# Kernel tuning notes

Hardware: AMD Instinct MI355X
Metric: run time of the kernel (lower is better)

## Reference

```python
import jax, jax.numpy as jnp
import numpy as np

SQ3, SQ5, SQ15 = 3.0**0.5, 5.0**0.5, 15.0**0.5
M0, M1, M2 = 128, 64, 32
DIM = M0 + 3*M1 + 5*M2  # 480
N_GRAPHS, ATOMS_PER, N_BLOCKS = 512, 16, 8
N_NODES = N_GRAPHS * ATOMS_PER
N_EDGES = 100000
CUTOFF = 5.0
AVG_DEGREE = 15.57
AVG_NUM_NODES = 18.03
ATOM_MAP = np.array([-1, 0, -1, -1, -1, -1, 1, 2, 3, 4], dtype=np.int32)


def _sph(u):
    # component-normalized real spherical harmonics l=1,2 of unit vectors u [E,3]
    x, y, z = u[:, 0], u[:, 1], u[:, 2]
    sh1 = SQ3 * u
    sh2 = jnp.stack([SQ15*x*y, SQ15*y*z, 0.5*SQ5*(3.0*z*z - 1.0),
                     SQ15*x*z, 0.5*SQ15*(x*x - y*y)], axis=-1)
    return sh1, sh2


def _seg_softmax(logits, seg, n):
    m = jax.ops.segment_max(logits, seg, num_segments=n)
    e = jnp.exp(logits - m[seg])
    s = jax.ops.segment_sum(e, seg, num_segments=n)
    return e / (s[seg] + 1e-9)


def _energy(pos, fp, node_atom, edge_src, edge_dst, batch):
    (atom_table, rbf_centers, rbf_width, deg_W1, deg_W2, deg_W3,
     blk_Wv0, blk_Wv1, blk_Wv2, blk_Ws0, blk_Ws1, blk_Ws2,
     blk_rW1, blk_rW2, blk_rW3, blk_Wa_src, blk_Wa_dst, blk_Wa_e, blk_wa,
     blk_ff1, blk_ff2, blk_fg1, blk_fg2, blk_fW1, blk_fW2,
     ln_g, ln_b, head_W0, head_out) = fp
    N = pos.shape[0]
    mapped = jnp.asarray(ATOM_MAP)[node_atom]
    f0 = atom_table[mapped]                       # [N,128] scalar channels
    f1 = jnp.zeros((N, M1, 3), f0.dtype)
    f2 = jnp.zeros((N, M2, 5), f0.dtype)

    vec = pos[edge_src] - pos[edge_dst]           # [E,3]
    r = jnp.sqrt(jnp.sum(vec*vec, axis=1) + 1e-12)
    u = vec / r[:, None]
    sh1, sh2 = _sph(u)
    rbf = jnp.exp(-0.5 * ((r[:, None] - rbf_centers[None, :]) / rbf_width[None, :])**2)  # [E,128]

    # edge-degree embedding: radial-weighted SH scattered to dst, scaled by avg degree
    h = jax.nn.silu(rbf @ deg_W1)
    h = jax.nn.silu(h @ deg_W2)
    g = h @ deg_W3                                 # [E,224]
    g0, g1, g2 = g[:, :M0], g[:, M0:M0+M1], g[:, M0+M1:]
    inv = 1.0 / (AVG_DEGREE ** 0.5)
    f0 = f0 + inv * jax.ops.segment_sum(g0, edge_dst, num_segments=N)
    f1 = f1 + inv * jax.ops.segment_sum(g1[:, :, None]*sh1[:, None, :], edge_dst, num_segments=N)
    f2 = f2 + inv * jax.ops.segment_sum(g2[:, :, None]*sh2[:, None, :], edge_dst, num_segments=N)

    for i in range(N_BLOCKS):
        s0, s1, s2 = f0[edge_src], f1[edge_src], f2[edge_src]
        h = jax.nn.silu(rbf @ blk_rW1[i])
        h = jax.nn.silu(h @ blk_rW2[i])
        g = h @ blk_rW3[i]
        g0, g1, g2 = g[:, :M0], g[:, M0:M0+M1], g[:, M0+M1:]
        # equivariant tensor-product messages: value path (radial-gated) + SH-injection path
        m0 = (s0 @ blk_Wv0[i]) * g0 + s0 @ blk_Ws0[i]
        m1 = jnp.einsum('ecx,cd->edx', s1, blk_Wv1[i]) * g1[:, :, None] \
             + (s0 @ blk_Ws1[i])[:, :, None] * sh1[:, None, :]
        m2 = jnp.einsum('ecx,cd->edx', s2, blk_Wv2[i]) * g2[:, :, None] \
             + (s0 @ blk_Ws2[i])[:, :, None] * sh2[:, None, :]
        # scalar attention, softmax over incoming edges per destination node
        z = jnp.tanh(s0 @ blk_Wa_src[i] + f0[edge_dst] @ blk_Wa_dst[i] + h @ blk_Wa_e[i])
        a = _seg_softmax(z @ blk_wa[i], edge_dst, N)  # [E]
        f0 = f0 + jax.ops.segment_sum(a[:, None]*m0, edge_dst, num_segments=N)
        f1 = f1 + jax.ops.segment_sum(a[:, None, None]*m1, edge_dst, num_segments=N)
        f2 = f2 + jax.ops.segment_sum(a[:, None, None]*m2, edge_dst, num_segments=N)
        # equivariant FFN: scalar MLP + scalar-gated per-l channel mixing
        f0 = f0 + jax.nn.silu(f0 @ blk_ff1[i]) @ blk_ff2[i]
        f1 = f1 + jnp.einsum('ncx,cd->ndx', f1, blk_fW1[i]) * jax.nn.sigmoid(f0 @ blk_fg1[i])[:, :, None]
        f2 = f2 + jnp.einsum('ncx,cd->ndx', f2, blk_fW2[i]) * jax.nn.sigmoid(f0 @ blk_fg2[i])[:, :, None]

    flat = jnp.concatenate([f0, f1.reshape(N, 3*M1), f2.reshape(N, 5*M2)], axis=1)  # [N,480]
    mu = jnp.mean(flat, axis=1, keepdims=True)
    var = jnp.var(flat, axis=1, keepdims=True)
    flat = (flat - mu) * jax.lax.rsqrt(var + 1e-5) * ln_g + ln_b
    # head: only the 0e part can reach the final 1x0e output (equivariance)
    e_node = jax.nn.silu(flat[:, :M0] @ head_W0) @ head_out  # [N,1]
    energy = jax.ops.segment_sum(e_node[:, 0], batch, num_segments=N_GRAPHS) / (AVG_NUM_NODES ** 0.5)
    return energy  # [B]


def setup_inputs() -> dict:
    key = jax.random.key(0)
    rng = np.random.default_rng(0)
    B, A = N_GRAPHS, ATOMS_PER
    pos_np = rng.uniform(0.0, 6.0, size=(B, A, 3)).astype(np.float32)
    d = np.linalg.norm(pos_np[:, :, None, :] - pos_np[:, None, :, :], axis=-1)
    mask = (d < CUTOFF) & (d > 1e-6)
    gi, si, di = np.nonzero(mask)
    src = np.resize((gi*A + si).astype(np.int32), N_EDGES)
    dst = np.resize((gi*A + di).astype(np.int32), N_EDGES)
    atoms = rng.choice(np.array([1, 6, 7, 8, 9], dtype=np.int32), size=B*A)
    batch = np.repeat(np.arange(B, dtype=np.int32), A)

    ks = iter(jax.random.split(key, 40))
    def W(shape, fan):
        return jax.random.normal(next(ks), shape, jnp.float32) / np.sqrt(fan)
    D3 = M0 + M1 + M2  # 224
    return dict(
        pos=jnp.asarray(pos_np.reshape(B*A, 3)),
        atom_table=W((5, M0), 1.0),
        rbf_centers=jnp.linspace(0.0, CUTOFF, 128),
        rbf_width=jnp.full((128,), 0.25, jnp.float32),
        deg_W1=W((128, 64), 128), deg_W2=W((64, 64), 64), deg_W3=W((64, D3), 64),
        blk_Wv0=W((8, M0, M0), M0), blk_Wv1=W((8, M1, M1), M1), blk_Wv2=W((8, M2, M2), M2),
        blk_Ws0=W((8, M0, M0), M0), blk_Ws1=W((8, M0, M1), M0), blk_Ws2=W((8, M0, M2), M0),
        blk_rW1=W((8, 128, 64), 128), blk_rW2=W((8, 64, 64), 64), blk_rW3=W((8, 64, D3), 64),
        blk_Wa_src=W((8, M0, 32), M0), blk_Wa_dst=W((8, M0, 32), M0), blk_Wa_e=W((8, 64, 32), 64),
        blk_wa=W((8, 32), 32),
        blk_ff1=W((8, M0, 4*M0), M0), blk_ff2=W((8, 4*M0, M0), 4*M0),
        blk_fg1=W((8, M0, M1), M0), blk_fg2=W((8, M0, M2), M0),
        blk_fW1=W((8, M1, M1), M1), blk_fW2=W((8, M2, M2), M2),
        ln_g=jnp.ones((DIM,), jnp.float32), ln_b=jnp.zeros((DIM,), jnp.float32),
        head_W0=W((M0, M0), M0), head_out=W((M0, 1), M0),
        node_atom=jnp.asarray(atoms), edge_src=jnp.asarray(src),
        edge_dst=jnp.asarray(dst), batch=jnp.asarray(batch),
    )


def reference(pos, atom_table, rbf_centers, rbf_width, deg_W1, deg_W2, deg_W3,
              blk_Wv0, blk_Wv1, blk_Wv2, blk_Ws0, blk_Ws1, blk_Ws2,
              blk_rW1, blk_rW2, blk_rW3, blk_Wa_src, blk_Wa_dst, blk_Wa_e, blk_wa,
              blk_ff1, blk_ff2, blk_fg1, blk_fg2, blk_fW1, blk_fW2,
              ln_g, ln_b, head_W0, head_out,
              node_atom, edge_src, edge_dst, batch):
    fp = (atom_table, rbf_centers, rbf_width, deg_W1, deg_W2, deg_W3,
          blk_Wv0, blk_Wv1, blk_Wv2, blk_Ws0, blk_Ws1, blk_Ws2,
          blk_rW1, blk_rW2, blk_rW3, blk_Wa_src, blk_Wa_dst, blk_Wa_e, blk_wa,
          blk_ff1, blk_ff2, blk_fg1, blk_fg2, blk_fW1, blk_fW2,
          ln_g, ln_b, head_W0, head_out)

    def _tot(p):
        e = _energy(p, fp, node_atom, edge_src, edge_dst, batch)
        return jnp.sum(e), e

    (_, energy), gpos = jax.value_and_grad(_tot, has_aux=True)(pos)
    forces = -gpos  # dy = -dE/dpos, as in the torch autograd.grad call
    return energy, forces
```

## Files before the change

kernel.cpp:

```cpp
#include <hip/hip_runtime.h>
#include <string.h>
#include <math.h>

#define NE 100000
#define NN 8192
#define NG 512
#define CHF 25000
#define NF 4
#define CHB 20000
#define NB 5
#define CHIF 50000
#define NIF 2
#define CHIB 34000
#define NIB 3
#define NNC 8192

#define SQ3F  1.7320508075688772f
#define SQ5F  2.23606797749979f
#define SQ15F 3.872983346207417f

__constant__ int c_amap[10] = {-1,0,-1,-1,-1,-1,1,2,3,4};

typedef __attribute__((ext_vector_type(4))) float f32x4;
typedef __attribute__((ext_vector_type(8))) short bf16x8;

__device__ __forceinline__ float sigf(float x){ return 1.0f/(1.0f+expf(-x)); }
__device__ __forceinline__ float siluf(float x){ return x*sigf(x); }
__device__ __forceinline__ float dsiluf(float x){ float s=sigf(x); return s*(1.0f + x*(1.0f-s)); }

__device__ __forceinline__ float wred64(float v){
  #pragma unroll
  for (int o=32;o>0;o>>=1) v += __shfl_down(v,o,64);
  return v;
}
__device__ __forceinline__ int lbound(const int* a, int n, int v){
  int lo=0, hi=n;
  while (lo<hi){ int m=(lo+hi)>>1; if (a[m]<v) lo=m+1; else hi=m; }
  return lo;
}
__device__ __forceinline__ unsigned short f2b(float x){
  unsigned u=__float_as_uint(x);
  unsigned r=(u + 0x7fffu + ((u>>16)&1u))>>16;
  return (unsigned short)r;
}
__device__ __forceinline__ float b2f(unsigned short b){
  return __uint_as_float(((unsigned)b)<<16);
}

__global__ void k_hist(const int* keys, int* hist, int n){
  int i = blockIdx.x*256 + threadIdx.x;
  if (i < n) atomicAdd(&hist[keys[i]], 1);
}
__global__ __launch_bounds__(256) void k_scan0(const int* hist, int* rows){
  __shared__ int part[256];
  int t = threadIdx.x;
  int base = t*32;
  int loc[32];
  int s = 0;
  #pragma unroll
  for (int i=0;i<32;i++){ loc[i]=s; s+=hist[base+i]; }
  part[t]=s;
  __syncthreads();
  int pre=0;
  for (int i=0;i<t;i++) pre+=part[i];
  #pragma unroll
  for (int i=0;i<32;i++) rows[base+i]=pre+loc[i];
  if (t==255) rows[NN]=pre+s;
}
__global__ void k_fillperm(const int* keys, int* cursor, int* perm, int n){
  int i = blockIdx.x*256 + threadIdx.x;
  if (i < n){
    int slot = atomicAdd(&cursor[keys[i]], 1);
    perm[slot] = i;
  }
}
__global__ void k_mkedge(const int* perm, const int* src, const int* dst, int* src2, int* dst2){
  int k = blockIdx.x*256 + threadIdx.x;
  if (k < NE){ int e = perm[k]; src2[k] = src[e]; dst2[k] = dst[e]; }
}

__global__ void k_wcat(const float* Wv0,const float* Ws0,const float* Ws1,const float* Ws2, float* W){
  int t = blockIdx.x*256 + threadIdx.x;
  if (t >= 8*128*352) return;
  int i = t/45056, r = t - i*45056;
  int k = r/352, n = r - k*352;
  float v;
  if (n < 128) v = Wv0[(size_t)i*16384 + k*128 + n];
  else if (n < 256) v = Ws0[(size_t)i*16384 + k*128 + (n-128)];
  else if (n < 320) v = Ws1[(size_t)i*8192 + k*64 + (n-256)];
  else v = Ws2[(size_t)i*4096 + k*32 + (n-320)];
  W[t] = v;
}
__global__ void k_wcatz(const float* WaS,const float* WaD,const float* WaE, float* W){
  int t = blockIdx.x*256 + threadIdx.x;
  if (t >= 8*320*32) return;
  int i = t/10240, r = t - i*10240;
  int k = r/32, c = r - k*32;
  float v;
  if (k < 128) v = WaS[(size_t)i*4096 + k*32 + c];
  else if (k < 256) v = WaD[(size_t)i*4096 + (k-128)*32 + c];
  else v = WaE[(size_t)i*2048 + (k-256)*32 + c];
  W[t] = v;
}
__global__ void k_wcatg(const float* fg1,const float* fg2, float* W){
  int t = blockIdx.x*256 + threadIdx.x;
  if (t >= 8*128*96) return;
  int i = t/12288, r = t - i*12288;
  int k = r/96, c = r - k*96;
  float v;
  if (c < 64) v = fg1[(size_t)i*8192 + k*64 + c];
  else v = fg2[(size_t)i*4096 + k*32 + (c-64)];
  W[t] = v;
}

template<int MT, bool TB, bool ACC, int ACT, bool GATHER, bool SPLIT, bool ARBF, bool DMUL, bool PREOUT>
__global__ __launch_bounds__(256) void k_mgemm(
    const float* __restrict__ A, const int* __restrict__ idx,
    const float* __restrict__ B, float* __restrict__ C,
    int M, int Nd, int K,
    const float* __restrict__ cen, const float* __restrict__ wid,
    const float* __restrict__ dm, float* __restrict__ pre)
{
  constexpr int TPR = 256/MT;
  constexpr int EPT = 32/TPR;
  constexpr int RT  = MT/16;
  __shared__ unsigned short Asb[(SPLIT?2:1)*MT*40];
  __shared__ unsigned short Btb[(SPLIT?2:1)*2560];
  const int bm = blockIdx.x*MT, bn = blockIdx.y*64;
  const int tid = threadIdx.x;
  const int wave = tid>>6, lane = tid&63;
  const int arow_s = tid / TPR, aoff = (tid % TPR) * EPT;
  const int bsrow = tid>>2, bsoff = (tid&3)*8;
  f32x4 acc[RT];
  #pragma unroll
  for (int r=0;r<RT;r++) acc[r] = (f32x4){0.f,0.f,0.f,0.f};
  int arow = -1;
  {
    int gr = bm + arow_s;
    if (gr < M) arow = GATHER ? idx[gr] : gr;
  }
  int bcol = bn + bsrow;
  for (int k0=0;k0<K;k0+=32){
    #pragma unroll
    for (int i=0;i<EPT;i++){
      float v = 0.0f;
      if (arow>=0){
        if (ARBF){
          float r = A[arow];
          int kk = k0 + aoff + i;
          float t = (r - cen[kk]) / wid[kk];
          v = expf(-0.5f*t*t);
        } else {
          v = A[(size_t)arow*K + k0 + aoff + i];
        }
      }
      unsigned short h = f2b(v);
      Asb[arow_s*40 + aoff + i] = h;
      if (SPLIT) Asb[MT*40 + arow_s*40 + aoff + i] = f2b(v - b2f(h));
    }
    #pragma unroll
    for (int i=0;i<8;i++){
      float v = 0.0f;
      if (bcol < Nd) v = TB ? B[(size_t)bcol*K + k0 + bsoff + i] : B[(size_t)(k0+bsoff+i)*Nd + bcol];
      unsigned short h = f2b(v);
      Btb[bsrow*40 + bsoff + i] = h;
      if (SPLIT) Btb[2560 + bsrow*40 + bsoff + i] = f2b(v - b2f(h));
    }
    __syncthreads();
    int boff = (wave*16 + (lane&15))*40 + (lane>>4)*8;
    bf16x8 bh = *(const bf16x8*)&Btb[boff];
    #pragma unroll
    for (int r=0;r<RT;r++){
      int aoff2 = (r*16 + (lane&15))*40 + (lane>>4)*8;
      bf16x8 ah = *(const bf16x8*)&Asb[aoff2];
      acc[r] = __builtin_amdgcn_mfma_f32_16x16x32_bf16(ah, bh, acc[r], 0,0,0);
      if (SPLIT){
        bf16x8 bl = *(const bf16x8*)&Btb[2560 + boff];
        bf16x8 al = *(const bf16x8*)&Asb[MT*40 + aoff2];
        acc[r] = __builtin_amdgcn_mfma_f32_16x16x32_bf16(ah, bl, acc[r], 0,0,0);
        acc[r] = __builtin_amdgcn_mfma_f32_16x16x32_bf16(al, bh, acc[r], 0,0,0);
      }
    }
    __syncthreads();
  }
  int col = bn + wave*16 + (lane&15);
  if (col < Nd){
    #pragma unroll
    for (int r=0;r<RT;r++){
      #pragma unroll
      for (int v=0;v<4;v++){
        int row = bm + r*16 + (lane>>4)*4 + v;
        if (row >= M) continue;
        size_t o = (size_t)row*Nd + col;
        float x = acc[r][v];
        if (ACC) x += C[o];
        if (DMUL) x *= dsiluf(dm[o]);
        if (PREOUT) pre[o] = x;
        if (ACT == 1) x = siluf(x);
        else if (ACT == 2) x = tanhf(x);
        else if (ACT == 3) x = sigf(x);
        C[o] = x;
      }
    }
  }
}

template<bool SPLIT, bool LAMB>
__global__ __launch_bounds__(256) void k_zgemm(
    const float* __restrict__ F0, const int* __restrict__ sidx, const int* __restrict__ didx,
    const float* __restrict__ H2v, const float* __restrict__ WZ, const float* __restrict__ wa,
    float* __restrict__ Zc, float* __restrict__ LAM, int M)
{
  __shared__ unsigned short Asb[(SPLIT?2:1)*64*40];
  __shared__ unsigned short Btb[(SPLIT?2:1)*2560];
  __shared__ float lacc[128];
  const int bm = blockIdx.x*64;
  const int tid = threadIdx.x, wave = tid>>6, lane = tid&63;
  const int arow_s = tid>>2, aoff = (tid&3)*8;
  const int bsrow = tid>>2, bsoff = (tid&3)*8;
  f32x4 acc[4];
  #pragma unroll
  for (int r=0;r<4;r++) acc[r] = (f32x4){0.f,0.f,0.f,0.f};
  long sb=-1, db=-1, hb=-1;
  {
    int gr = bm + arow_s;
    if (gr < M){ sb=(long)sidx[gr]*128; db=(long)didx[gr]*128; hb=(long)gr*64; }
  }
  for (int k0=0;k0<320;k0+=32){
    long ab; int rk; const float* sp;
    if (k0 < 128){ ab=sb; rk=k0; sp=F0; }
    else if (k0 < 256){ ab=db; rk=k0-128; sp=F0; }
    else { ab=hb; rk=k0-256; sp=H2v; }
    #pragma unroll
    for (int i=0;i<8;i++){
      float v = (ab>=0) ? sp[ab + rk + aoff + i] : 0.0f;
      unsigned short h = f2b(v);
      Asb[arow_s*40 + aoff + i] = h;
      if (SPLIT) Asb[64*40 + arow_s*40 + aoff + i] = f2b(v - b2f(h));
    }
    #pragma unroll
    for (int i=0;i<8;i++){
      int kk = k0 + bsoff + i;
      float v = (bsrow < 32) ? WZ[kk*32 + bsrow] : 0.0f;
      unsigned short h = f2b(v);
      Btb[bsrow*40 + bsoff + i] = h;
      if (SPLIT) Btb[2560 + bsrow*40 + bsoff + i] = f2b(v - b2f(h));
    }
    __syncthreads();
    int boff = (wave*16 + (lane&15))*40 + (lane>>4)*8;
    bf16x8 bh = *(const bf16x8*)&Btb[boff];
    #pragma unroll
    for (int r=0;r<4;r++){
      int aoff2 = (r*16 + (lane&15))*40 + (lane>>4)*8;
      bf16x8 ah = *(const bf16x8*)&Asb[aoff2];
      acc[r] = __builtin_amdgcn_mfma_f32_16x16x32_bf16(ah, bh, acc[r], 0,0,0);
      if (SPLIT){
        bf16x8 bl = *(const bf16x8*)&Btb[2560 + boff];
        bf16x8 al = *(const bf16x8*)&Asb[64*40 + aoff2];
        acc[r] = __builtin_amdgcn_mfma_f32_16x16x32_bf16(ah, bl, acc[r], 0,0,0);
        acc[r] = __builtin_amdgcn_mfma_f32_16x16x32_bf16(al, bh, acc[r], 0,0,0);
      }
    }
    __syncthreads();
  }
  int col = wave*16 + (lane&15);
  if (wave < 2){
    #pragma unroll
    for (int r=0;r<4;r++){
      #pragma unroll
      for (int v=0;v<4;v++){
        int row = bm + r*16 + (lane>>4)*4 + v;
        float z = tanhf(acc[r][v]);
        if (row < M) Zc[(size_t)row*32 + col] = z;
        if (LAMB){
          float p = (row < M) ? z*wa[col] : 0.0f;
          #pragma unroll
          for (int o=8;o>0;o>>=1) p += __shfl_xor(p, o, 64);
          if ((lane&15)==0) lacc[wave*64 + r*16 + (lane>>4)*4 + v] = p;
        }
      }
    }
  }
  if (LAMB){
    __syncthreads();
    if (tid < 64){
      int row = bm + tid;
      if (row < M) LAM[row] = expf(lacc[tid] + lacc[64+tid]);
    }
  }
}

template<int CI, int CO, int X, bool TB, bool ACC, bool GATHER, bool SPLIT, bool GATE>
__global__ __launch_bounds__(256) void k_meinsum(
    const float* __restrict__ A, const int* __restrict__ idx,
    const float* __restrict__ W, float* __restrict__ C, int M,
    const float* __restrict__ P, int PS, int POFF)
{
  __shared__ unsigned short Asb[(SPLIT?2:1)*2560];
  __shared__ unsigned short Btb[(SPLIT?2:1)*2560];
  const int bm = blockIdx.x*64;
  const int tid = threadIdx.x, wave = tid>>6, lane = tid&63;
  const int srow = tid>>2, soff = (tid&3)*8;
  f32x4 acc[4];
  #pragma unroll
  for (int r=0;r<4;r++) acc[r] = (f32x4){0.f,0.f,0.f,0.f};
  long abase = -1;
  {
    int grow = bm + srow;
    if (grow < M*X){
      int ge = grow / X, gx = grow - ge*X;
      int ar = GATHER ? idx[ge] : ge;
      abase = (long)ar*CI*X + gx;
    }
  }
  for (int k0=0;k0<CI;k0+=32){
    #pragma unroll
    for (int i=0;i<8;i++){
      float v = (abase>=0) ? A[abase + (size_t)(k0+soff+i)*X] : 0.0f;
      unsigned short h = f2b(v);
      Asb[srow*40 + soff + i] = h;
      if (SPLIT) Asb[2560 + srow*40 + soff + i] = f2b(v - b2f(h));
    }
    #pragma unroll
    for (int i=0;i<8;i++){
      int kk = k0 + soff + i;
      float v = 0.0f;
      if (srow < CO) v = TB ? W[srow*CI + kk] : W[kk*CO + srow];
      unsigned short h = f2b(v);
      Btb[srow*40 + soff + i] = h;
      if (SPLIT) Btb[2560 + srow*40 + soff + i] = f2b(v - b2f(h));
    }
    __syncthreads();
    int boff = (wave*16 + (lane&15))*40 + (lane>>4)*8;
    bf16x8 bh = *(const bf16x8*)&Btb[boff];
    #pragma unroll
    for (int r=0;r<4;r++){
      int aoff = (r*16 + (lane&15))*40 + (lane>>4)*8;
      bf16x8 ah = *(const bf16x8*)&Asb[aoff];
      acc[r] = __builtin_amdgcn_mfma_f32_16x16x32_bf16(ah, bh, acc[r], 0,0,0);
      if (SPLIT){
        bf16x8 bl = *(const bf16x8*)&Btb[2560 + boff];
        bf16x8 al = *(const bf16x8*)&Asb[2560 + aoff];
        acc[r] = __builtin_amdgcn_mfma_f32_16x16x32_bf16(ah, bl, acc[r], 0,0,0);
        acc[r] = __builtin_amdgcn_mfma_f32_16x16x32_bf16(al, bh, acc[r], 0,0,0);
      }
    }
    __syncthreads();
  }
  int col = wave*16 + (lane&15);
  if (col < CO){
    #pragma unroll
    for (int r=0;r<4;r++){
      #pragma unroll
      for (int v=0;v<4;v++){
        int row = bm + r*16 + (lane>>4)*4 + v;
        if (row >= M*X) continue;
        int ge = row / X, gx = row - ge*X;
        size_t o = (size_t)ge*CO*X + (size_t)col*X + gx;
        float xx = acc[r][v];
        if (GATE){
          float p = P[(size_t)ge*PS + POFF + col];
          C[o] = A[o] + xx*p;
        } else {
          if (ACC) xx += C[o];
          C[o] = xx;
        }
      }
    }
  }
}

__global__ void k_sentinel(float* o, int n, float v){
  int i = blockIdx.x*256 + threadIdx.x;
  if (i < n) o[i] = v;
}

__global__ void k_geom(const float* __restrict__ pos, const int* __restrict__ src, const int* __restrict__ dst,
                       float* __restrict__ U, float* __restrict__ Rr, float* __restrict__ SH2b){
  int e = blockIdx.x*256 + threadIdx.x;
  if (e >= NE) return;
  int s = src[e], d = dst[e];
  float vx = pos[s*3+0]-pos[d*3+0];
  float vy = pos[s*3+1]-pos[d*3+1];
  float vz = pos[s*3+2]-pos[d*3+2];
  float r = sqrtf(vx*vx+vy*vy+vz*vz + 1e-12f);
  float ux=vx/r, uy=vy/r, uz=vz/r;
  U[e*3+0]=ux; U[e*3+1]=uy; U[e*3+2]=uz;
  Rr[e]=r;
  SH2b[e*5+0]=SQ15F*ux*uy;
  SH2b[e*5+1]=SQ15F*uy*uz;
  SH2b[e*5+2]=0.5f*SQ5F*(3.0f*uz*uz-1.0f);
  SH2b[e*5+3]=SQ15F*ux*uz;
  SH2b[e*5+4]=0.5f*SQ15F*(ux*ux-uy*uy);
}

__global__ void k_f0init(const int* __restrict__ na, const float* __restrict__ at, float* __restrict__ f0){
  int t = blockIdx.x*256 + threadIdx.x;
  if (t >= NN*128) return;
  int n = t>>7, j = t&127;
  int m = c_amap[na[n]];
  f0[t] = at[m*128+j];
}

__global__ void k_postblk(const float* __restrict__ x0,const float* __restrict__ x1,const float* __restrict__ x2,
                          float* __restrict__ y0,float* __restrict__ y1,float* __restrict__ y2,
                          const float* __restrict__ S, unsigned short* __restrict__ ck,
                          const float* __restrict__ Pl, const int* __restrict__ dst, float* __restrict__ AB){
  int t = blockIdx.x*256 + threadIdx.x;
  if (t < NE) AB[t] = Pl[t]/(S[dst[t]]+1e-9f);
  if (t >= NN*480) return;
  float v;
  if (t < NN*128){ int n=t>>7; v = x0[t] + y0[t]/(S[n]+1e-9f); y0[t]=v; }
  else if (t < NN*320){ int q=t-NN*128; int n=q/192; v = x1[q] + y1[q]/(S[n]+1e-9f); y1[q]=v; }
  else { int q=t-NN*320; int n=q/160; v = x2[q] + y2[q]/(S[n]+1e-9f); y2[q]=v; }
  ck[t] = f2b(v);
}

__global__ void k_q3(const float* __restrict__ f0,const float* __restrict__ f1,const float* __restrict__ f2,
                     unsigned short* __restrict__ ck){
  int t = blockIdx.x*256 + threadIdx.x;
  if (t >= NN*480) return;
  float v;
  if (t < NN*128) v = f0[t];
  else if (t < NN*320) v = f1[t-NN*128];
  else v = f2[t-NN*320];
  ck[t] = f2b(v);
}
__global__ void k_dq3x2(const unsigned short* __restrict__ cka, const unsigned short* __restrict__ ckb,
                        float* __restrict__ a0,float* __restrict__ a1,float* __restrict__ a2,
                        float* __restrict__ b0,float* __restrict__ b1,float* __restrict__ b2){
  int t = blockIdx.x*256 + threadIdx.x;
  if (t >= NN*480) return;
  float va = b2f(cka[t]), vb = b2f(ckb[t]);
  if (t < NN*128){ a0[t]=va; b0[t]=vb; }
  else if (t < NN*320){ int q=t-NN*128; a1[q]=va; b1[q]=vb; }
  else { int q=t-NN*320; a2[q]=va; b2[q]=vb; }
}

template<bool INIT>
__global__ __launch_bounds__(512) void k_agg(
  float* __restrict__ f0o,float* __restrict__ f1o,float* __restrict__ f2o,
  const float* __restrict__ SC,const float* __restrict__ sv1,const float* __restrict__ sv2,
  const float* __restrict__ g,const float* __restrict__ U,const float* __restrict__ SH2b,
  const float* __restrict__ aArr,const int* __restrict__ keys,const int* __restrict__ dst,
  float* __restrict__ SACC, int c0, int c1)
{
  __shared__ float acc[7680];
  int b = blockIdx.x, lo = b<<4;
  int e0 = lbound(keys, NE, lo), e1 = lbound(keys, NE, lo+16);
  if (e0 < c0) e0 = c0;
  if (e1 > c1) e1 = c1;
  if (e0 >= e1) return;
  for (int i=threadIdx.x;i<7680;i+=512) acc[i]=0.0f;
  __syncthreads();
  const int j = threadIdx.x;
  const float inv = 1.0f/sqrtf(15.57f);
  int cat=3, cc_=0, xx_=0;
  if (j<128){ cat=0; }
  else if (j<320){ cat=1; int t=j-128; cc_=t/3; xx_=t-3*cc_; }
  else if (j<480){ cat=2; int t=j-320; cc_=t/5; xx_=t-5*cc_; }
  float sacc=0.0f;
  for (int e=e0; e<e1; ++e){
    int el = e - c0;
    float a = INIT ? inv : aArr[e];
    int nl = dst[e]&15;
    if (cat==0){
      float m = INIT ? g[el*224+j] : (SC[(size_t)el*352+j]*g[el*224+j] + SC[(size_t)el*352+128+j]);
      acc[nl*480+j] += a*m;
    } else if (cat==1){
      int t=j-128;
      float sh = SQ3F*U[e*3+xx_];
      float m = INIT ? g[el*224+128+cc_]*sh : (sv1[el*192+t]*g[el*224+128+cc_] + SC[(size_t)el*352+256+cc_]*sh);
      acc[nl*480+j] += a*m;
    } else if (cat==2){
      int t=j-320;
      float sh = SH2b[e*5+xx_];
      float m = INIT ? g[el*224+192+cc_]*sh : (sv2[el*160+t]*g[el*224+192+cc_] + SC[(size_t)el*352+320+cc_]*sh);
      acc[nl*480+j] += a*m;
    } else if (!INIT && j<496){
      if (nl==(j-480)) sacc += a;
    }
  }
  __syncthreads();
  for (int i=threadIdx.x;i<7680;i+=512){
    int nl=i/480, jj=i-480*nl, n=lo+nl;
    float v=acc[i];
    if (jj<128) f0o[n*128+jj]+=v;
    else if (jj<320) f1o[n*192+jj-128]+=v;
    else f2o[n*160+jj-320]+=v;
  }
  if (!INIT && j>=480 && j<496) SACC[lo+(j-480)] += sacc;
}

__global__ __launch_bounds__(640) void k_scat(
  float* __restrict__ df0, float* __restrict__ df1, float* __restrict__ df2,
  const float* __restrict__ DE0, const float* __restrict__ DZD,
  const float* __restrict__ DE1, const float* __restrict__ DE2,
  const int* __restrict__ src, const int* __restrict__ dst, int c0, int c1)
{
  __shared__ float acc[7680];
  int b=blockIdx.x, lo=b<<4;
  int e0=lbound(dst,NE,lo), e1=lbound(dst,NE,lo+16);
  if (e0 < c0) e0 = c0;
  if (e1 > c1) e1 = c1;
  for (int i=threadIdx.x;i<7680;i+=640) acc[i]=0.0f;
  __syncthreads();
  const int j=threadIdx.x;
  for (int e=e0;e<e1;++e){
    int el=e-c0;
    int sl=(src[e]&15)*480, dl=(dst[e]&15)*480;
    if (j<128) acc[sl+j] += DE0[el*128+j];
    else if (j<256){ int q=j-128; acc[dl+q] += DZD[el*128+q]; }
    else if (j<448){ int q=j-256; acc[sl+128+q] += DE1[el*192+q]; }
    else if (j<608){ int q=j-448; acc[sl+320+q] += DE2[el*160+q]; }
    __syncthreads();
  }
  for (int i=threadIdx.x;i<7680;i+=640){
    int nl=i/480, jj=i-480*nl, n=lo+nl;
    float v=acc[i];
    if (jj<128) df0[n*128+jj]+=v;
    else if (jj<320) df1[n*192+jj-128]+=v;
    else df2[n*160+jj-320]+=v;
  }
}

__global__ __launch_bounds__(256) void k_ssum(
  const float* __restrict__ FA0,const float* __restrict__ FA1,const float* __restrict__ FA2,
  const float* __restrict__ FB0,const float* __restrict__ FB1,const float* __restrict__ FB2,
  const float* __restrict__ DY0,const float* __restrict__ DY1,const float* __restrict__ DY2,
  float* __restrict__ SSUM)
{
  int n=blockIdx.x*4+(threadIdx.x>>6), lane=threadIdx.x&63;
  if (n>=NN) return;
  float s=0.0f;
  for (int j=lane;j<480;j+=64){
    float d,g;
    if (j<128){ d=FB0[n*128+j]-FA0[n*128+j]; g=DY0[n*128+j]; }
    else if (j<320){ int q=j-128; d=FB1[n*192+q]-FA1[n*192+q]; g=DY1[n*192+q]; }
    else { int q=j-320; d=FB2[n*160+q]-FA2[n*160+q]; g=DY2[n*160+q]; }
    s += d*g;
  }
  s = wred64(s);
  if (lane==0) SSUM[n]=s;
}

__global__ __launch_bounds__(256) void k_bedge(
  float* __restrict__ SC, float* __restrict__ SV1, float* __restrict__ SV2,
  const float* __restrict__ g, const float* __restrict__ U, const float* __restrict__ SH2b,
  const float* __restrict__ df0,const float* __restrict__ df1,const float* __restrict__ df2,
  const int* __restrict__ dst, const float* __restrict__ SSUM, const float* __restrict__ wa,
  float* __restrict__ Z, const float* __restrict__ aArr,
  float* __restrict__ DG, float* __restrict__ DSH1, float* __restrict__ DSH2,
  int c0, int cnt)
{
  int w=threadIdx.x>>6, lane=threadIdx.x&63;
  int el=blockIdx.x*4+w;
  if (el>=cnt) return;
  int e=c0+el;
  int d=dst[e];
  float s=0.0f;
  for (int j=lane;j<480;j+=64){
    float m, dfv;
    if (j<128){
      m = SC[(size_t)el*352+j]*g[el*224+j] + SC[(size_t)el*352+128+j];
      dfv = df0[(size_t)d*128+j];
    } else if (j<320){
      int t=j-128, c=t/3, x=t-3*c;
      m = SV1[el*192+t]*g[el*224+128+c] + SC[(size_t)el*352+256+c]*(SQ3F*U[e*3+x]);
      dfv = df1[(size_t)d*192+t];
    } else {
      int t=j-320, c=t/5, x=t-5*c;
      m = SV2[el*160+t]*g[el*224+192+c] + SC[(size_t)el*352+320+c]*SH2b[e*5+x];
      dfv = df2[(size_t)d*160+t];
    }
    s += m*dfv;
  }
  s = wred64(s);
  s = __shfl(s,0,64);
  float a = aArr[e];
  float dlam = a*(s - SSUM[d]);
  if (lane<32){
    float z = Z[(size_t)el*32+lane];
    Z[(size_t)el*32+lane] = dlam*wa[lane]*(1.0f-z*z);
  }
  {
    float* row = SC + (size_t)el*352;
    for (int j=lane;j<128;j+=64){
      float dm = a*df0[(size_t)d*128+j];
      float sv = row[j];
      row[128+j] = dm;
      row[j] = dm*g[el*224+j];
      DG[el*224+j] = dm*sv;
    }
  }
  {
    float dm0=a*df1[(size_t)d*192+lane*3+0];
    float dm1=a*df1[(size_t)d*192+lane*3+1];
    float dm2=a*df1[(size_t)d*192+lane*3+2];
    float sw1o=SC[(size_t)el*352+256+lane];
    float g1=g[el*224+128+lane];
    float c0v=dm0*sw1o, c1v=dm1*sw1o, c2v=dm2*sw1o;
    c0v=wred64(c0v); c1v=wred64(c1v); c2v=wred64(c2v);
    if (lane==0){ DSH1[e*3+0]+=c0v; DSH1[e*3+1]+=c1v; DSH1[e*3+2]+=c2v; }
    float sh0=SQ3F*U[e*3+0], sh1=SQ3F*U[e*3+1], sh2=SQ3F*U[e*3+2];
    SC[(size_t)el*352+256+lane]=dm0*sh0+dm1*sh1+dm2*sh2;
    float sv0o=SV1[el*192+lane*3+0], sv1o=SV1[el*192+lane*3+1], sv2o=SV1[el*192+lane*3+2];
    DG[el*224+128+lane]=dm0*sv0o+dm1*sv1o+dm2*sv2o;
    SV1[el*192+lane*3+0]=dm0*g1; SV1[el*192+lane*3+1]=dm1*g1; SV1[el*192+lane*3+2]=dm2*g1;
  }
  {
    float dm[5]={0,0,0,0,0}, svo[5]={0,0,0,0,0};
    float sw2o=0.0f, g2=0.0f;
    if (lane<32){
      #pragma unroll
      for (int x=0;x<5;x++){ dm[x]=a*df2[(size_t)d*160+lane*5+x]; svo[x]=SV2[el*160+lane*5+x]; }
      sw2o=SC[(size_t)el*352+320+lane]; g2=g[el*224+192+lane];
    }
    float c[5];
    #pragma unroll
    for (int x=0;x<5;x++){ c[x]=dm[x]*sw2o; c[x]=wred64(c[x]); }
    if (lane==0){
      #pragma unroll
      for (int x=0;x<5;x++) DSH2[e*5+x]+=c[x];
    }
    if (lane<32){
      float dsw=0.0f, dg2=0.0f;
      #pragma unroll
      for (int x=0;x<5;x++){ dsw+=dm[x]*SH2b[e*5+x]; dg2+=dm[x]*svo[x]; }
      SC[(size_t)el*352+320+lane]=dsw;
      DG[el*224+192+lane]=dg2;
      #pragma unroll
      for (int x=0;x<5;x++) SV2[el*160+lane*5+x]=dm[x]*g2;
    }
  }
}

template<int CD,int X>
__global__ void k_gateback(const float* __restrict__ dfB, float* __restrict__ V,
                           const float* __restrict__ P12, float* __restrict__ DPa, int poff){
  int t=blockIdx.x*256+threadIdx.x;
  if (t>=NN*CD) return;
  int n=t/CD, d=t-n*CD;
  float p=P12[(size_t)n*96+poff+d];
  float dp=0.0f;
  #pragma unroll
  for (int x=0;x<X;x++){ dp += dfB[(size_t)t*X+x]*V[(size_t)t*X+x]; }
  #pragma unroll
  for (int x=0;x<X;x++){ V[(size_t)t*X+x] = dfB[(size_t)t*X+x]*p; }
  DPa[(size_t)n*96+poff+d] = dp*p*(1.0f-p);
}

__global__ __launch_bounds__(256) void k_dr(const float* __restrict__ DRBF, const float* __restrict__ Rr,
    const float* __restrict__ cen, const float* __restrict__ wid, float* __restrict__ DRa, int c0, int cnt){
  int w=threadIdx.x>>6, lane=threadIdx.x&63;
  int el=blockIdx.x*4+w;
  if (el>=cnt) return;
  int e=c0+el;
  float r=Rr[e], s=0.0f;
  for (int k=lane;k<128;k+=64){
    float c=cen[k], wd=wid[k];
    float t=(r-c)/wd;
    float rb=expf(-0.5f*t*t);
    s += DRBF[el*128+k]*rb*((c-r)/(wd*wd));
  }
  s=wred64(s);
  if (lane==0) DRa[e]+=s;
}

__global__ __launch_bounds__(256) void k_initback(
  const float* __restrict__ df0,const float* __restrict__ df1,const float* __restrict__ df2,
  const int* __restrict__ dst,
  const float* __restrict__ g,const float* __restrict__ U,const float* __restrict__ SH2b,
  float* __restrict__ DG,float* __restrict__ DSH1,float* __restrict__ DSH2, int c0, int cnt)
{
  int w=threadIdx.x>>6, lane=threadIdx.x&63;
  int el=blockIdx.x*4+w;
  if (el>=cnt) return;
  int e=c0+el;
  int d=dst[e];
  const float inv=1.0f/sqrtf(15.57f);
  for (int j=lane;j<128;j+=64) DG[el*224+j]=inv*df0[d*128+j];
  float sh0=SQ3F*U[e*3+0], sh1=SQ3F*U[e*3+1], sh2=SQ3F*U[e*3+2];
  float df10=df1[d*192+lane*3+0], df11=df1[d*192+lane*3+1], df12=df1[d*192+lane*3+2];
  float g1=g[el*224+128+lane];
  DG[el*224+128+lane]=inv*(df10*sh0+df11*sh1+df12*sh2);
  float c0v=g1*df10, c1v=g1*df11, c2v=g1*df12;
  c0v=wred64(c0v); c1v=wred64(c1v); c2v=wred64(c2v);
  if (lane==0){ DSH1[e*3+0]+=inv*c0v; DSH1[e*3+1]+=inv*c1v; DSH1[e*3+2]+=inv*c2v; }
  float cc[5]={0,0,0,0,0};
  if (lane<32){
    float g2=g[el*224+192+lane];
    float dgv=0.0f;
    #pragma unroll
    for (int x=0;x<5;x++){ float dfv=df2[d*160+lane*5+x]; dgv+=dfv*SH2b[e*5+x]; cc[x]=g2*dfv; }
    DG[el*224+192+lane]=inv*dgv;
  }
  #pragma unroll
  for (int x=0;x<5;x++) cc[x]=wred64(cc[x]);
  if (lane==0){
    #pragma unroll
    for (int x=0;x<5;x++) DSH2[e*5+x]+=inv*cc[x];
  }
}

__global__ void k_geoback(const float* __restrict__ DRa, const float* __restrict__ DSH1, const float* __restrict__ DSH2,
                          const float* __restrict__ U, const float* __restrict__ Rr,
                          const int* __restrict__ src, const int* __restrict__ dst,
                          float* __restrict__ DPOS){
  int e=blockIdx.x*256+threadIdx.x;
  if (e>=NE) return;
  float ux=U[e*3+0], uy=U[e*3+1], uz=U[e*3+2];
  float r=Rr[e];
  float dux=SQ3F*DSH1[e*3+0], duy=SQ3F*DSH1[e*3+1], duz=SQ3F*DSH1[e*3+2];
  float d0=DSH2[e*5+0],d1=DSH2[e*5+1],d2=DSH2[e*5+2],d3=DSH2[e*5+3],d4=DSH2[e*5+4];
  dux += SQ15F*(uy*d0+uz*d3+ux*d4);
  duy += SQ15F*(ux*d0+uz*d1-uy*d4);
  duz += SQ15F*(uy*d1+ux*d3)+3.0f*SQ5F*uz*d2;
  float dr=DRa[e];
  float dot=dux*ux+duy*uy+duz*uz;
  float dvx=(dux-dot*ux)/r+dr*ux;
  float dvy=(duy-dot*uy)/r+dr*uy;
  float dvz=(duz-dot*uz)/r+dr*uz;
  int s=src[e], d=dst[e];
  atomicAdd(&DPOS[s*3+0],dvx); atomicAdd(&DPOS[s*3+1],dvy); atomicAdd(&DPOS[s*3+2],dvz);
  atomicAdd(&DPOS[d*3+0],-dvx); atomicAdd(&DPOS[d*3+1],-dvy); atomicAdd(&DPOS[d*3+2],-dvz);
}

__global__ void k_forces(const float* __restrict__ DPOS, float* __restrict__ o){
  int i=blockIdx.x*256+threadIdx.x;
  if (i<NN*3) o[i]=-DPOS[i];
}

__global__ __launch_bounds__(64) void k_lnhead(
  const float* __restrict__ f0,const float* __restrict__ f1,const float* __restrict__ f2,
  const float* __restrict__ lng,const float* __restrict__ lnb,
  const float* __restrict__ W0,const float* __restrict__ hout,
  float* __restrict__ EN, float* __restrict__ df0,float* __restrict__ df1,float* __restrict__ df2)
{
  __shared__ float xh[480];
  __shared__ float fl[128];
  __shared__ float dyv[128];
  __shared__ float dxh[128];
  int n=blockIdx.x, lane=threadIdx.x;
  const float c0=1.0f/sqrtf(18.03f);
  for (int i=lane;i<480;i+=64){
    float v=(i<128)? f0[n*128+i] : (i<320)? f1[n*192+(i-128)] : f2[n*160+(i-320)];
    xh[i]=v;
  }
  __syncthreads();
  float s1=0.0f,s2=0.0f;
  for (int i=lane;i<480;i+=64){ float v=xh[i]; s1+=v; s2+=v*v; }
  s1=wred64(s1); s2=wred64(s2);
  float mu=__shfl(s1,0,64)*(1.0f/480.0f);
  float var=__shfl(s2,0,64)*(1.0f/480.0f)-mu*mu;
  float rstd=rsqrtf(var+1e-5f);
  for (int i=lane;i<480;i+=64) xh[i]=(xh[i]-mu)*rstd;
  __syncthreads();
  for (int k=lane;k<128;k+=64) fl[k]=xh[k]*lng[k]+lnb[k];
  __syncthreads();
  float y0=0.0f,y1=0.0f;
  for (int k=0;k<128;k++){ float f=fl[k]; y0+=f*W0[k*128+lane]; y1+=f*W0[k*128+lane+64]; }
  float e = siluf(y0)*hout[lane] + siluf(y1)*hout[lane+64];
  e=wred64(e);
  if (lane==0) EN[n]=e*c0;
  dyv[lane]=c0*hout[lane]*dsiluf(y0);
  dyv[lane+64]=c0*hout[lane+64]*dsiluf(y1);
  __syncthreads();
  float d0=0.0f,d1=0.0f;
  for (int j=0;j<128;j++){ float dv=dyv[j]; d0+=dv*W0[lane*128+j]; d1+=dv*W0[(lane+64)*128+j]; }
  dxh[lane]=d0*lng[lane];
  dxh[lane+64]=d1*lng[lane+64];
  __syncthreads();
  float s3=dxh[lane]+dxh[lane+64];
  float s4=dxh[lane]*xh[lane]+dxh[lane+64]*xh[lane+64];
  s3=wred64(s3); s4=wred64(s4);
  float m1=__shfl(s3,0,64)*(1.0f/480.0f);
  float m2=__shfl(s4,0,64)*(1.0f/480.0f);
  for (int i=lane;i<480;i+=64){
    float dv=rstd*(((i<128)?dxh[i]:0.0f)-m1-xh[i]*m2);
    if (i<128) df0[n*128+i]=dv;
    else if (i<320) df1[n*192+(i-128)]=dv;
    else df2[n*160+(i-320)]=dv;
  }
}

__global__ void k_esum(const float* __restrict__ EN, float* __restrict__ out){
  int b=blockIdx.x*64+threadIdx.x;
  if (b<NG){
    float s=0.0f;
    for (int k=0;k<16;k++) s+=EN[b*16+k];
    out[b]=s;
  }
}

#define MG(MT,TB,ACC,ACT,GA,SP,AR,DM,PO, A,IDX,B,C,M,Nd,K, CEN,WID,DMp,POp) \
  k_mgemm<MT,TB,ACC,ACT,GA,SP,AR,DM,PO><<<dim3((unsigned)(((M)+(MT)-1)/(MT)),(unsigned)(((Nd)+63)/64)),dim3(256),0,stream>>>((A),(IDX),(B),(C),(M),(Nd),(K),(CEN),(WID),(DMp),(POp))
#define MGEMM(MT,TB,ACC,ACT,GA, A,IDX,B,C,M,Nd,K) MG(MT,TB,ACC,ACT,GA,false,false,false,false, A,IDX,B,C,M,Nd,K, nullptr,nullptr,nullptr,nullptr)
#define MGEMM3(MT,TB,ACC,ACT,GA, A,IDX,B,C,M,Nd,K) MG(MT,TB,ACC,ACT,GA,true,false,false,false, A,IDX,B,C,M,Nd,K, nullptr,nullptr,nullptr,nullptr)
#define MEINS(CI,CO,X,TB,ACC,GA, A,IDX,Wt,C,M) \
  k_meinsum<CI,CO,X,TB,ACC,GA,false,false><<<dim3((unsigned)(((M)*(X)+63)/64)),dim3(256),0,stream>>>((A),(IDX),(Wt),(C),(M),nullptr,0,0)
#define MEINS3(CI,CO,X,TB,ACC,GA, A,IDX,Wt,C,M) \
  k_meinsum<CI,CO,X,TB,ACC,GA,true,false><<<dim3((unsigned)(((M)*(X)+63)/64)),dim3(256),0,stream>>>((A),(IDX),(Wt),(C),(M),nullptr,0,0)
#define MEINSG(CI,CO,X,SP, A,Wt,C,M, Pp,POFF) \
  k_meinsum<CI,CO,X,false,false,false,SP,true><<<dim3((unsigned)(((M)*(X)+63)/64)),dim3(256),0,stream>>>((A),nullptr,(Wt),(C),(M),(Pp),96,(POFF))
#define G256(n) dim3((unsigned)(((n)+255)/256)),dim3(256),0,stream
#define GW4(n) dim3((unsigned)(((n)+3)/4)),dim3(256),0,stream

extern "C" void kernel_launch(void* const* d_in, const int* in_sizes, int n_in,
                              void* d_out, int out_size, void* d_ws, size_t ws_size,
                              hipStream_t stream)
{
  const float* pos =(const float*)d_in[0];
  const float* atab=(const float*)d_in[1];
  const float* rbfc=(const float*)d_in[2];
  const float* rbfw=(const float*)d_in[3];
  const float* degW1=(const float*)d_in[4];
  const float* degW2=(const float*)d_in[5];
  const float* degW3=(const float*)d_in[6];
  const float* Wv0=(const float*)d_in[7];
  const float* Wv1=(const float*)d_in[8];
  const float* Wv2=(const float*)d_in[9];
  const float* Ws0=(const float*)d_in[10];
  const float* Ws1=(const float*)d_in[11];
  const float* Ws2=(const float*)d_in[12];
  const float* rW1=(const float*)d_in[13];
  const float* rW2=(const float*)d_in[14];
  const float* rW3=(const float*)d_in[15];
  const float* WaS=(const float*)d_in[16];
  const float* WaD=(const float*)d_in[17];
  const float* WaE=(const float*)d_in[18];
  const float* wab=(const float*)d_in[19];
  const float* ff1=(const float*)d_in[20];
  const float* ff2=(const float*)d_in[21];
  const float* fg1=(const float*)d_in[22];
  const float* fg2=(const float*)d_in[23];
  const float* fW1=(const float*)d_in[24];
  const float* fW2=(const float*)d_in[25];
  const float* lng=(const float*)d_in[26];
  const float* lnb=(const float*)d_in[27];
  const float* W0h=(const float*)d_in[28];
  const float* hout=(const float*)d_in[29];
  const int* natom=(const int*)d_in[30];
  const int* esrc=(const int*)d_in[31];
  const int* edst=(const int*)d_in[32];

  float* Wp=(float*)d_ws;
  size_t off=0;
  auto al=[&](size_t n)->float*{ float* q=Wp+off; off+=n; return q; };

  const size_t SLOT = (size_t)NN*480;
  unsigned short* CKB = (unsigned short*)al((9*SLOT+1)/2);
  float* FA0=al((size_t)NN*128); float* FA1=al((size_t)NN*192); float* FA2=al((size_t)NN*160);
  float* FB0=al((size_t)NN*128); float* FB1=al((size_t)NN*192); float* FB2=al((size_t)NN*160);
  float* DI0=al((size_t)NN*128); float* DI1=al((size_t)NN*192); float* DI2=al((size_t)NN*160);
  float* DY0=al((size_t)NN*128); float* DY1=al((size_t)NN*192); float* DY2=al((size_t)NN*160);
  float* U=al((size_t)NE*3); float* Rr=al(NE); float* SH2b=al((size_t)NE*5);
  float* ABLK=al(8ULL*NE); float* LAM=al(NE);
  float* SSUM=al(NN); float* ENODE=al(NN); float* SACC=al(NN);
  float* DRr=al(NE); float* DSH1=al((size_t)NE*3); float* DSH2=al((size_t)NE*5);
  float* DPOS=al((size_t)NN*3);
  float* WCATF=al(8ULL*128*352);
  float* WCATZ=al(8ULL*320*32);
  float* WCATG=al(8ULL*128*96);
  int* ROWS =(int*)al(NN+1);
  int* CNT  =(int*)al(NN);
  int* POSB =(int*)al(NN);
  int* PERMB=(int*)al(NE);
  int* ESRC2=(int*)al(NE);
  int* EDST2=(int*)al(NE);

  const size_t UNI = 28800000;
  float* UN = al(UNI);
  float* TBc=UN;
  float* DTc=TBc+(size_t)NNC*512;
  float* P12=DTc+(size_t)NNC*512;
  float* V1 =P12+(size_t)NN*96;
  float* V2 =V1 +(size_t)NN*192;
  float* DPb=V2 +(size_t)NN*160;
  float* F0N=DPb+(size_t)NN*96;

  float* outE=(float*)d_out;
  float* outF=outE+NG;

  if (off*sizeof(float) > ws_size){
    k_sentinel<<<G256(out_size)>>>(outE, out_size, (float)ws_size);
    return;
  }

  (void)hipMemsetAsync(CNT,0,NN*sizeof(int),stream);
  k_hist<<<G256(NE)>>>(edst,CNT,NE);
  k_scan0<<<dim3(1),dim3(256),0,stream>>>(CNT,ROWS);
  (void)hipMemcpyAsync(POSB,ROWS,NN*sizeof(int),hipMemcpyDeviceToDevice,stream);
  k_fillperm<<<G256(NE)>>>(edst,POSB,PERMB,NE);
  k_mkedge<<<G256(NE)>>>(PERMB,esrc,edst,ESRC2,EDST2);
  k_wcat<<<G256(8*128*352)>>>(Wv0,Ws0,Ws1,Ws2,WCATF);
  k_wcatz<<<G256(8*320*32)>>>(WaS,WaD,WaE,WCATZ);
  k_wcatg<<<G256(8*128*96)>>>(fg1,fg2,WCATG);

  k_geom<<<G256(NE)>>>(pos,ESRC2,EDST2,U,Rr,SH2b);
  k_f0init<<<G256(NN*128)>>>(natom,atab,FA0);
  (void)hipMemsetAsync(FA1,0,(size_t)NN*352*4,stream);
  (void)hipMemsetAsync(DRr,0,(size_t)NE*4,stream);
  (void)hipMemsetAsync(DSH1,0,(size_t)NE*3*4,stream);
  (void)hipMemsetAsync(DSH2,0,(size_t)NE*5*4,stream);
  (void)hipMemsetAsync(DPOS,0,(size_t)NN*3*4,stream);

  {
    float* H1=UN; float* H2=H1+(size_t)CHIF*64; float* Gc=H2+(size_t)CHIF*64;
    for (int cc=0;cc<NIF;cc++){
      int c0e=cc*CHIF, cnt=(c0e+CHIF<=NE)?CHIF:(NE-c0e);
      MG(64,false,false,1,false, true,true,false,false, Rr+c0e,nullptr,degW1,H1, cnt,64,128, rbfc,rbfw,nullptr,nullptr);
      MGEMM3(64,false,false,1,false, H1,nullptr,degW2,H2, cnt,64,64);
      MGEMM3(64,false,false,0,false, H2,nullptr,degW3,Gc, cnt,224,64);
      k_agg<true><<<dim3(NG),dim3(512),0,stream>>>(FA0,FA1,FA2,
        nullptr,nullptr,nullptr, Gc,U,SH2b, nullptr, EDST2,EDST2, nullptr, c0e,c0e+cnt);
    }
  }
  k_q3<<<G256(NN*480)>>>(FA0,FA1,FA2, CKB);

  float *c0_=FA0,*c1_=FA1,*c2_=FA2, *n0_=FB0,*n1_=FB1,*n2_=FB2;

  {
    float* H1  =UN;
    float* H2  =H1  +(size_t)CHF*64;
    float* Gc  =H2  +(size_t)CHF*64;
    float* SCAT=Gc  +(size_t)CHF*224;
    float* SV1 =SCAT+(size_t)CHF*352;
    float* SV2 =SV1 +(size_t)CHF*192;
    float* Zc  =SV2 +(size_t)CHF*160;
    for (int i=0;i<8;i++){
      const float* Wv1i=Wv1+(size_t)i*4096; const float* Wv2i=Wv2+(size_t)i*1024;
      const float* rW1i=rW1+(size_t)i*8192; const float* rW2i=rW2+(size_t)i*4096; const float* rW3i=rW3+(size_t)i*14336;
      const float* WZi=WCATZ+(size_t)i*10240;
      const float* ff1i=ff1+(size_t)i*65536; const float* ff2i=ff2+(size_t)i*65536;
      const float* fgCi=WCATG+(size_t)i*12288;
      const float* fW1i=fW1+(size_t)i*4096; const float* fW2i=fW2+(size_t)i*1024;
      const float* WCi=WCATF+(size_t)i*45056;
      float* AB=ABLK+(size_t)i*NE;

      (void)hipMemsetAsync(SACC,0,(size_t)NN*4,stream);
      (void)hipMemsetAsync(n0_,0,(size_t)NN*128*4,stream);
      (void)hipMemsetAsync(n1_,0,(size_t)NN*352*4,stream);
      for (int cc=0;cc<NF;cc++){
        int c0e=cc*CHF, cnt=(c0e+CHF<=NE)?CHF:(NE-c0e);
        MG(64,false,false,1,false, true,true,false,false, Rr+c0e,nullptr,rW1i,H1, cnt,64,128, rbfc,rbfw,nullptr,nullptr);
        MGEMM3(64,false,false,1,false, H1,nullptr,rW2i,H2, cnt,64,64);
        MGEMM3(64,false,false,0,false, H2,nullptr,rW3i,Gc, cnt,224,64);
        k_zgemm<true,true><<<dim3((unsigned)((cnt+63)/64)),dim3(256),0,stream>>>(
            c0_, ESRC2+c0e, EDST2+c0e, H2, WZi, wab+(size_t)i*32, Zc, LAM+c0e, cnt);
        MGEMM3(64,false,false,0,true, c0_,ESRC2+c0e,WCi,SCAT, cnt,352,128);
        MEINS3(64,64,3,false,false,true, c1_,ESRC2+c0e,Wv1i,SV1, cnt);
        MEINS3(32,32,5,false,false,true, c2_,ESRC2+c0e,Wv2i,SV2, cnt);
        k_agg<false><<<dim3(NG),dim3(512),0,stream>>>(n0_,n1_,n2_,
          SCAT,SV1,SV2, Gc,U,SH2b, LAM, EDST2,EDST2, SACC, c0e,c0e+cnt);
      }
      k_postblk<<<G256(NN*480)>>>(c0_,c1_,c2_, n0_,n1_,n2_, SACC, CKB+(size_t)(i+1)*SLOT, LAM, EDST2, AB);
      for (int nc=0;nc<NN/NNC;nc++){
        MGEMM3(64,false,false,1,false, n0_+(size_t)nc*NNC*128,nullptr,ff1i,TBc, NNC,512,128);
        MGEMM3(64,false,true, 0,false, TBc,nullptr,ff2i, n0_+(size_t)nc*NNC*128, NNC,128,512);
      }
      MGEMM3(64,false,false,3,false, n0_,nullptr,fgCi,P12, NN,96,128);
      MEINSG(64,64,3,true, n1_,fW1i,c1_, NN, P12, 0);
      MEINSG(32,32,5,true, n2_,fW2i,c2_, NN, P12, 64);
      float* t;
      t=c0_;c0_=n0_;n0_=t;
    }
  }

  k_lnhead<<<dim3(NN),dim3(64),0,stream>>>(c0_,c1_,c2_, lng,lnb,W0h,hout, ENODE, DI0,DI1,DI2);
  k_esum<<<dim3(8),dim3(64),0,stream>>>(ENODE,outE);

  {
    float* PRE1=UN;
    float* PRE2=PRE1+(size_t)CHB*64;
    float* H1  =PRE2+(size_t)CHB*64;
    float* H2  =H1  +(size_t)CHB*64;
    float* Gc  =H2  +(size_t)CHB*64;
    float* DGc =Gc  +(size_t)CHB*224;
    float* SCAT=DGc +(size_t)CHB*224;
    float* SV1 =SCAT+(size_t)CHB*352;
    float* SV2 =SV1 +(size_t)CHB*192;
    float* Zc  =SV2 +(size_t)CHB*160;
    float* DE0 =PRE1;
    float* RBFc=DGc;
    float* DZD =Gc;
    for (int i=7;i>=0;--i){
      const float* Wv1i=Wv1+(size_t)i*4096; const float* Wv2i=Wv2+(size_t)i*1024;
      const float* rW1i=rW1+(size_t)i*8192; const float* rW2i=rW2+(size_t)i*4096; const float* rW3i=rW3+(size_t)i*14336;
      const float* WZi=WCATZ+(size_t)i*10240;
      const float* WaSi=WaS+(size_t)i*4096; const float* WaDi=WaD+(size_t)i*4096; const float* WaEi=WaE+(size_t)i*2048;
      const float* ff1i=ff1+(size_t)i*65536; const float* ff2i=ff2+(size_t)i*65536;
      const float* fgCi=WCATG+(size_t)i*12288;
      const float* fW1i=fW1+(size_t)i*4096; const float* fW2i=fW2+(size_t)i*1024;
      const float* WCi=WCATF+(size_t)i*45056;
      const float* AB=ABLK+(size_t)i*NE;
      float *fa1=FA1, *fa2=FA2, *dy1=DY1, *dy2=DY2;

      k_dq3x2<<<G256(NN*480)>>>(CKB+(size_t)i*SLOT, CKB+(size_t)(i+1)*SLOT, FA0,FA1,FA2, FB0,FB1,FB2);
      if (i>0){
        const float* pf1=ff1+(size_t)(i-1)*65536; const float* pf2=ff2+(size_t)(i-1)*65536;
        const float* pgC=WCATG+(size_t)(i-1)*12288;
        const float* pW1=fW1+(size_t)(i-1)*4096; const float* pW2=fW2+(size_t)(i-1)*1024;
        for (int nc=0;nc<NN/NNC;nc++){
          MGEMM(64,false,false,1,false, FA0+(size_t)nc*NNC*128,nullptr,pf1,TBc, NNC,512,128);
          MGEMM(64,false,true, 0,false, TBc,nullptr,pf2, FA0+(size_t)nc*NNC*128, NNC,128,512);
        }
        MGEMM(64,false,false,3,false, FA0,nullptr,pgC,P12, NN,96,128);
        MEINSG(64,64,3,false, FA1,pW1,DY1, NN, P12, 0);
        MEINSG(32,32,5,false, FA2,pW2,DY2, NN, P12, 64);
        fa1=DY1; dy1=FA1; fa2=DY2; dy2=FA2;
      }
      (void)hipMemcpyAsync(F0N,FB0,(size_t)NN*128*4,hipMemcpyDeviceToDevice,stream);
      for (int nc=0;nc<NN/NNC;nc++){
        MGEMM(64,false,false,1,false, FB0+(size_t)nc*NNC*128,nullptr,ff1i,TBc, NNC,512,128);
        MGEMM(64,false,true, 0,false, TBc,nullptr,ff2i, F0N+(size_t)nc*NNC*128, NNC,128,512);
      }
      MGEMM(64,false,false,3,false, F0N,nullptr,fgCi,P12, NN,96,128);
      MEINS(64,64,3,false,false,false, FB1,nullptr,fW1i,V1, NN);
      MEINS(32,32,5,false,false,false, FB2,nullptr,fW2i,V2, NN);
      k_gateback<64,3><<<G256(NN*64)>>>(DI1,V1,P12,DPb,0);
      k_gateback<32,5><<<G256(NN*32)>>>(DI2,V2,P12,DPb,64);
      MGEMM(64,true,true,0,false, DPb,nullptr,fgCi,DI0, NN,128,96);
      (void)hipMemcpyAsync(dy1,DI1,(size_t)NN*192*4,hipMemcpyDeviceToDevice,stream);
      MEINS(64,64,3,true,true,false, V1,nullptr,fW1i,dy1, NN);
      (void)hipMemcpyAsync(dy2,DI2,(size_t)NN*160*4,hipMemcpyDeviceToDevice,stream);
      MEINS(32,32,5,true,true,false, V2,nullptr,fW2i,dy2, NN);
      (void)hipMemcpyAsync(DY0,DI0,(size_t)NN*128*4,hipMemcpyDeviceToDevice,stream);
      for (int nc=0;nc<NN/NNC;nc++){
        MGEMM(64,false,false,0,false, FB0+(size_t)nc*NNC*128,nullptr,ff1i,TBc, NNC,512,128);
        MG(64,true,false,0,false, false,false,true,false, DI0+(size_t)nc*NNC*128,nullptr,ff2i,DTc, NNC,512,128, nullptr,nullptr,TBc,nullptr);
        MGEMM(64,true,true,0,false, DTc,nullptr,ff1i, DY0+(size_t)nc*NNC*128, NNC,128,512);
      }
      k_ssum<<<dim3(NN/4),dim3(256),0,stream>>>(FA0,fa1,fa2,FB0,FB1,FB2,DY0,dy1,dy2,SSUM);
      (void)hipMemcpyAsync(DI0,DY0,(size_t)NN*128*4,hipMemcpyDeviceToDevice,stream);
      (void)hipMemcpyAsync(DI1,dy1,(size_t)NN*192*4,hipMemcpyDeviceToDevice,stream);
      (void)hipMemcpyAsync(DI2,dy2,(size_t)NN*160*4,hipMemcpyDeviceToDevice,stream);
      for (int cc=0;cc<NB;cc++){
        int c0e=cc*CHB, cnt=(c0e+CHB<=NE)?CHB:(NE-c0e);
        MG(64,false,false,1,false, false,true,false,true, Rr+c0e,nullptr,rW1i,H1, cnt,64,128, rbfc,rbfw,nullptr,PRE1);
        MG(64,false,false,1,false, false,false,false,true, H1,nullptr,rW2i,H2, cnt,64,64, nullptr,nullptr,nullptr,PRE2);
        MGEMM(64,false,false,0,false, H2,nullptr,rW3i,Gc, cnt,224,64);
        k_zgemm<false,false><<<dim3((unsigned)((cnt+63)/64)),dim3(256),0,stream>>>(
            FA0, ESRC2+c0e, EDST2+c0e, H2, WZi, nullptr, Zc, nullptr, cnt);
        MGEMM(64,false,false,0,true, FA0,ESRC2+c0e,WCi,SCAT, cnt,352,128);
        MEINS(64,64,3,false,false,true, fa1,ESRC2+c0e,Wv1i,SV1, cnt);
        MEINS(32,32,5,false,false,true, fa2,ESRC2+c0e,Wv2i,SV2, cnt);
        k_bedge<<<GW4(cnt)>>>(SCAT,SV1,SV2, Gc,U,SH2b, DY0,dy1,dy2, EDST2, SSUM,
                              wab+(size_t)i*32, Zc, AB, DGc, DSH1, DSH2, c0e, cnt);
        MGEMM(64,true,false,0,false, Zc,nullptr,WaEi,H2, cnt,64,32);
        MG(64,true,true,0,false, false,false,true,false, DGc,nullptr,rW3i,H2, cnt,64,224, nullptr,nullptr,PRE2,nullptr);
        MG(64,true,false,0,false, false,false,true,false, H2,nullptr,rW2i,H1, cnt,64,64, nullptr,nullptr,PRE1,nullptr);
        MGEMM(64,true,false,0,false, H1,nullptr,rW1i,RBFc, cnt,128,64);
        k_dr<<<GW4(cnt)>>>(RBFc,Rr,rbfc,rbfw,DRr, c0e,cnt);
        MGEMM(64,true,false,0,false, SCAT,nullptr,WCi,DE0, cnt,128,352);
        MGEMM(64,true,true, 0,false, Zc,nullptr,WaSi,DE0, cnt,128,32);
        MGEMM(64,true,false,0,false, Zc,nullptr,WaDi,DZD, cnt,128,32);
        MEINS(64,64,3,true,false,false, SV1,nullptr,Wv1i,SV1, cnt);
        MEINS(32,32,5,true,false,false, SV2,nullptr,Wv2i,SV2, cnt);
        k_scat<<<dim3(NG),dim3(640),0,stream>>>(DI0,DI1,DI2, DE0,DZD,SV1,SV2, ESRC2,EDST2, c0e,c0e+cnt);
      }
    }
  }

  {
    float* PRE1=UN;
    float* PRE2=PRE1+(size_t)CHIB*64;
    float* H1  =PRE2+(size_t)CHIB*64;
    float* H2  =H1  +(size_t)CHIB*64;
    float* Gc  =H2  +(size_t)CHIB*64;
    float* DGc =Gc  +(size_t)CHIB*224;
    float* RBFc=DGc +(size_t)CHIB*224;
    for (int cc=0;cc<NIB;cc++){
      int c0e=cc*CHIB, cnt=(c0e+CHIB<=NE)?CHIB:(NE-c0e);
      MG(64,false,false,1,false, false,true,false,true, Rr+c0e,nullptr,degW1,H1, cnt,64,128, rbfc,rbfw,nullptr,PRE1);
      MG(64,false,false,1,false, false,false,false,true, H1,nullptr,degW2,H2, cnt,64,64, nullptr,nullptr,nullptr,PRE2);
      MGEMM(64,false,false,0,false, H2,nullptr,degW3,Gc, cnt,224,64);
      k_initback<<<GW4(cnt)>>>(DI0,DI1,DI2,EDST2,Gc,U,SH2b,DGc,DSH1,DSH2, c0e,cnt);
      MG(64,true,false,0,false, false,false,true,false, DGc,nullptr,degW3,H2, cnt,64,224, nullptr,nullptr,PRE2,nullptr);
      MG(64,true,false,0,false, false,false,true,false, H2,nullptr,degW2,H1, cnt,64,64, nullptr,nullptr,PRE1,nullptr);
      MGEMM(64,true,false,0,false, H1,nullptr,degW1,RBFc, cnt,128,64);
      k_dr<<<GW4(cnt)>>>(RBFc,Rr,rbfc,rbfw,DRr, c0e,cnt);
    }
  }

  k_geoback<<<G256(NE)>>>(DRr,DSH1,DSH2,U,Rr,ESRC2,EDST2,DPOS);
  k_forces<<<G256(NN*3)>>>(DPOS,outF);
  (void)in_sizes; (void)n_in; (void)out_size;
}
```

Before: 31.58 ms.

## Pre-quantize weights to bf16 hi/lo once and size edge chunks from workspace

```diff
diff --git a/kernel.cpp b/kernel.cpp
--- a/kernel.cpp
+++ b/kernel.cpp
@@ -5,14 +5,6 @@
 #define NE 100000
 #define NN 8192
 #define NG 512
-#define CHF 25000
-#define NF 4
-#define CHB 20000
-#define NB 5
-#define CHIF 50000
-#define NIF 2
-#define CHIB 34000
-#define NIB 3
 #define NNC 8192
 
 #define SQ3F  1.7320508075688772f
@@ -79,7 +71,16 @@
   if (k < NE){ int e = perm[k]; src2[k] = src[e]; dst2[k] = dst[e]; }
 }
 
-__global__ void k_wcat(const float* Wv0,const float* Ws0,const float* Ws1,const float* Ws2, float* W){
+__global__ void k_qw(const float* __restrict__ src, unsigned short* __restrict__ dst, int tot, int n){
+  int i = blockIdx.x*256 + threadIdx.x;
+  if (i >= n) return;
+  float v = src[i];
+  unsigned short h = f2b(v);
+  dst[i] = h;
+  if (tot) dst[i+tot] = f2b(v - b2f(h));
+}
+__global__ void k_wcatfq(const float* Wv0,const float* Ws0,const float* Ws1,const float* Ws2,
+                         unsigned short* __restrict__ q){
   int t = blockIdx.x*256 + threadIdx.x;
   if (t >= 8*128*352) return;
   int i = t/45056, r = t - i*45056;
@@ -89,9 +90,10 @@
   else if (n < 256) v = Ws0[(size_t)i*16384 + k*128 + (n-128)];
   else if (n < 320) v = Ws1[(size_t)i*8192 + k*64 + (n-256)];
   else v = Ws2[(size_t)i*4096 + k*32 + (n-320)];
-  W[t] = v;
-}
-__global__ void k_wcatz(const float* WaS,const float* WaD,const float* WaE, float* W){
+  unsigned short h = f2b(v);
+  q[t] = h; q[t+360448] = f2b(v - b2f(h));
+}
+__global__ void k_wcatzq(const float* WaS,const float* WaD,const float* WaE, unsigned short* __restrict__ q){
   int t = blockIdx.x*256 + threadIdx.x;
   if (t >= 8*320*32) return;
   int i = t/10240, r = t - i*10240;
@@ -100,9 +102,10 @@
   if (k < 128) v = WaS[(size_t)i*4096 + k*32 + c];
   else if (k < 256) v = WaD[(size_t)i*4096 + (k-128)*32 + c];
   else v = WaE[(size_t)i*2048 + (k-256)*32 + c];
-  W[t] = v;
-}
-__global__ void k_wcatg(const float* fg1,const float* fg2, float* W){
+  unsigned short h = f2b(v);
+  q[t] = h; q[t+81920] = f2b(v - b2f(h));
+}
+__global__ void k_wcatgq(const float* fg1,const float* fg2, unsigned short* __restrict__ q){
   int t = blockIdx.x*256 + threadIdx.x;
   if (t >= 8*128*96) return;
   int i = t/12288, r = t - i*12288;
@@ -110,16 +113,17 @@
   float v;
   if (c < 64) v = fg1[(size_t)i*8192 + k*64 + c];
   else v = fg2[(size_t)i*4096 + k*32 + (c-64)];
-  W[t] = v;
+  unsigned short h = f2b(v);
+  q[t] = h; q[t+98304] = f2b(v - b2f(h));
 }
 
 template<int MT, bool TB, bool ACC, int ACT, bool GATHER, bool SPLIT, bool ARBF, bool DMUL, bool PREOUT>
 __global__ __launch_bounds__(256) void k_mgemm(
     const float* __restrict__ A, const int* __restrict__ idx,
-    const float* __restrict__ B, float* __restrict__ C,
+    const unsigned short* __restrict__ Bh, int blo, float* __restrict__ C,
     int M, int Nd, int K,
     const float* __restrict__ cen, const float* __restrict__ wid,
-    const float* __restrict__ dm, float* __restrict__ pre)
+    const float* __restrict__ dm, float* __restrict__ pre, const float* __restrict__ Dacc)
 {
   constexpr int TPR = 256/MT;
   constexpr int EPT = 32/TPR;
@@ -160,11 +164,15 @@
     }
     #pragma unroll
     for (int i=0;i<8;i++){
-      float v = 0.0f;
-      if (bcol < Nd) v = TB ? B[(size_t)bcol*K + k0 + bsoff + i] : B[(size_t)(k0+bsoff+i)*Nd + bcol];
-      unsigned short h = f2b(v);
+      int kk = k0 + bsoff + i;
+      unsigned short h = 0, l = 0;
+      if (bcol < Nd){
+        size_t bi = TB ? ((size_t)bcol*K + kk) : ((size_t)kk*Nd + bcol);
+        h = Bh[bi];
+        if (SPLIT) l = Bh[bi + (size_t)blo];
+      }
       Btb[bsrow*40 + bsoff + i] = h;
-      if (SPLIT) Btb[2560 + bsrow*40 + bsoff + i] = f2b(v - b2f(h));
+      if (SPLIT) Btb[2560 + bsrow*40 + bsoff + i] = l;
     }
     __syncthreads();
     int boff = (wave*16 + (lane&15))*40 + (lane>>4)*8;
@@ -193,7 +201,7 @@
         if (row >= M) continue;
         size_t o = (size_t)row*Nd + col;
         float x = acc[r][v];
-        if (ACC) x += C[o];
+        if (ACC) x += (Dacc ? Dacc[o] : C[o]);
         if (DMUL) x *= dsiluf(dm[o]);
         if (PREOUT) pre[o] = x;
         if (ACT == 1) x = siluf(x);
@@ -208,7 +216,8 @@
 template<bool SPLIT, bool LAMB>
 __global__ __launch_bounds__(256) void k_zgemm(
     const float* __restrict__ F0, const int* __restrict__ sidx, const int* __restrict__ didx,
-    const float* __restrict__ H2v, const float* __restrict__ WZ, const float* __restrict__ wa,
+    const float* __restrict__ H2v, const unsigned short* __restrict__ WZh, int zlo,
+    const float* __restrict__ wa,
     float* __restrict__ Zc, float* __restrict__ LAM, int M)
 {
   __shared__ unsigned short Asb[(SPLIT?2:1)*64*40];
@@ -241,10 +250,14 @@
     #pragma unroll
     for (int i=0;i<8;i++){
       int kk = k0 + bsoff + i;
-      float v = (bsrow < 32) ? WZ[kk*32 + bsrow] : 0.0f;
-      unsigned short h = f2b(v);
+      unsigned short h=0, l=0;
+      if (bsrow < 32){
+        size_t bi = (size_t)kk*32 + bsrow;
+        h = WZh[bi];
+        if (SPLIT) l = WZh[bi + (size_t)zlo];
+      }
       Btb[bsrow*40 + bsoff + i] = h;
-      if (SPLIT) Btb[2560 + bsrow*40 + bsoff + i] = f2b(v - b2f(h));
+      if (SPLIT) Btb[2560 + bsrow*40 + bsoff + i] = l;
     }
     __syncthreads();
     int boff = (wave*16 + (lane&15))*40 + (lane>>4)*8;
@@ -293,8 +306,8 @@
 template<int CI, int CO, int X, bool TB, bool ACC, bool GATHER, bool SPLIT, bool GATE>
 __global__ __launch_bounds__(256) void k_meinsum(
     const float* __restrict__ A, const int* __restrict__ idx,
-    const float* __restrict__ W, float* __restrict__ C, int M,
-    const float* __restrict__ P, int PS, int POFF)
+    const unsigned short* __restrict__ Wh, int wlo, float* __restrict__ C, int M,
+    const float* __restrict__ P, int PS, int POFF, const float* __restrict__ Dacc)
 {
   __shared__ unsigned short Asb[(SPLIT?2:1)*2560];
   __shared__ unsigned short Btb[(SPLIT?2:1)*2560];
@@ -324,11 +337,14 @@
     #pragma unroll
     for (int i=0;i<8;i++){
       int kk = k0 + soff + i;
-      float v = 0.0f;
-      if (srow < CO) v = TB ? W[srow*CI + kk] : W[kk*CO + srow];
-      unsigned short h = f2b(v);
+      unsigned short h=0, l=0;
+      if (srow < CO){
+        size_t bi = TB ? ((size_t)srow*CI + kk) : ((size_t)kk*CO + srow);
+        h = Wh[bi];
+        if (SPLIT) l = Wh[bi + (size_t)wlo];
+      }
       Btb[srow*40 + soff + i] = h;
-      if (SPLIT) Btb[2560 + srow*40 + soff + i] = f2b(v - b2f(h));
+      if (SPLIT) Btb[2560 + srow*40 + soff + i] = l;
     }
     __syncthreads();
     int boff = (wave*16 + (lane&15))*40 + (lane>>4)*8;
@@ -362,7 +378,7 @@
           float p = P[(size_t)ge*PS + POFF + col];
           C[o] = A[o] + xx*p;
         } else {
-          if (ACC) xx += C[o];
+          if (ACC) xx += (Dacc ? Dacc[o] : C[o]);
           C[o] = xx;
         }
       }
@@ -793,16 +809,19 @@
   }
 }
 
-#define MG(MT,TB,ACC,ACT,GA,SP,AR,DM,PO, A,IDX,B,C,M,Nd,K, CEN,WID,DMp,POp) \
-  k_mgemm<MT,TB,ACC,ACT,GA,SP,AR,DM,PO><<<dim3((unsigned)(((M)+(MT)-1)/(MT)),(unsigned)(((Nd)+63)/64)),dim3(256),0,stream>>>((A),(IDX),(B),(C),(M),(Nd),(K),(CEN),(WID),(DMp),(POp))
-#define MGEMM(MT,TB,ACC,ACT,GA, A,IDX,B,C,M,Nd,K) MG(MT,TB,ACC,ACT,GA,false,false,false,false, A,IDX,B,C,M,Nd,K, nullptr,nullptr,nullptr,nullptr)
-#define MGEMM3(MT,TB,ACC,ACT,GA, A,IDX,B,C,M,Nd,K) MG(MT,TB,ACC,ACT,GA,true,false,false,false, A,IDX,B,C,M,Nd,K, nullptr,nullptr,nullptr,nullptr)
-#define MEINS(CI,CO,X,TB,ACC,GA, A,IDX,Wt,C,M) \
-  k_meinsum<CI,CO,X,TB,ACC,GA,false,false><<<dim3((unsigned)(((M)*(X)+63)/64)),dim3(256),0,stream>>>((A),(IDX),(Wt),(C),(M),nullptr,0,0)
-#define MEINS3(CI,CO,X,TB,ACC,GA, A,IDX,Wt,C,M) \
-  k_meinsum<CI,CO,X,TB,ACC,GA,true,false><<<dim3((unsigned)(((M)*(X)+63)/64)),dim3(256),0,stream>>>((A),(IDX),(Wt),(C),(M),nullptr,0,0)
-#define MEINSG(CI,CO,X,SP, A,Wt,C,M, Pp,POFF) \
-  k_meinsum<CI,CO,X,false,false,false,SP,true><<<dim3((unsigned)(((M)*(X)+63)/64)),dim3(256),0,stream>>>((A),nullptr,(Wt),(C),(M),(Pp),96,(POFF))
+#define MG(MT,TB,ACC,ACT,GA,SP,AR,DM,PO, A,IDX,BH,BL,C,M,Nd,K, CEN,WID,DMp,POp,DAp) \
+  k_mgemm<MT,TB,ACC,ACT,GA,SP,AR,DM,PO><<<dim3((unsigned)(((M)+(MT)-1)/(MT)),(unsigned)(((Nd)+63)/64)),dim3(256),0,stream>>>((A),(IDX),(BH),(BL),(C),(M),(Nd),(K),(CEN),(WID),(DMp),(POp),(DAp))
+#define MGEMM(MT,TB,ACC,ACT,GA, A,IDX,BH,BL,C,M,Nd,K) MG(MT,TB,ACC,ACT,GA,false,false,false,false, A,IDX,BH,BL,C,M,Nd,K, nullptr,nullptr,nullptr,nullptr,nullptr)
+#define MGEMMD(MT,TB,ACC,ACT,GA, A,IDX,BH,BL,C,M,Nd,K,DA) MG(MT,TB,ACC,ACT,GA,false,false,false,false, A,IDX,BH,BL,C,M,Nd,K, nullptr,nullptr,nullptr,nullptr,DA)
+#define MGEMM3(MT,TB,ACC,ACT,GA, A,IDX,BH,BL,C,M,Nd,K) MG(MT,TB,ACC,ACT,GA,true,false,false,false, A,IDX,BH,BL,C,M,Nd,K, nullptr,nullptr,nullptr,nullptr,nullptr)
+#define MEINS(CI,CO,X,TB,ACC,GA, A,IDX,WH,WL,C,M) \
+  k_meinsum<CI,CO,X,TB,ACC,GA,false,false><<<dim3((unsigned)(((M)*(X)+63)/64)),dim3(256),0,stream>>>((A),(IDX),(WH),(WL),(C),(M),nullptr,0,0,nullptr)
+#define MEINSD(CI,CO,X,TB,ACC,GA, A,IDX,WH,WL,C,M,DA) \
+  k_meinsum<CI,CO,X,TB,ACC,GA,false,false><<<dim3((unsigned)(((M)*(X)+63)/64)),dim3(256),0,stream>>>((A),(IDX),(WH),(WL),(C),(M),nullptr,0,0,(DA))
+#define MEINS3(CI,CO,X,TB,ACC,GA, A,IDX,WH,WL,C,M) \
+  k_meinsum<CI,CO,X,TB,ACC,GA,true,false><<<dim3((unsigned)(((M)*(X)+63)/64)),dim3(256),0,stream>>>((A),(IDX),(WH),(WL),(C),(M),nullptr,0,0,nullptr)
+#define MEINSG(CI,CO,X,SP, A,WH,WL,C,M, Pp,POFF) \
+  k_meinsum<CI,CO,X,false,false,false,SP,true><<<dim3((unsigned)(((M)*(X)+63)/64)),dim3(256),0,stream>>>((A),nullptr,(WH),(WL),(C),(M),(Pp),96,(POFF),nullptr)
 #define G256(n) dim3((unsigned)(((n)+255)/256)),dim3(256),0,stream
 #define GW4(n) dim3((unsigned)(((n)+3)/4)),dim3(256),0,stream
 
@@ -856,21 +875,62 @@
   float* DY0=al((size_t)NN*128); float* DY1=al((size_t)NN*192); float* DY2=al((size_t)NN*160);
   float* U=al((size_t)NE*3); float* Rr=al(NE); float* SH2b=al((size_t)NE*5);
   float* ABLK=al(8ULL*NE); float* LAM=al(NE);
-  float* SSUM=al(NN); float* ENODE=al(NN); float* SACC=al(NN);
+  float* SSUM=al(NN); float* SACC=al(NN);
+  float* ENODE=SSUM;
   float* DRr=al(NE); float* DSH1=al((size_t)NE*3); float* DSH2=al((size_t)NE*5);
   float* DPOS=al((size_t)NN*3);
-  float* WCATF=al(8ULL*128*352);
-  float* WCATZ=al(8ULL*320*32);
-  float* WCATG=al(8ULL*128*96);
   int* ROWS =(int*)al(NN+1);
   int* CNT  =(int*)al(NN);
-  int* POSB =(int*)al(NN);
-  int* PERMB=(int*)al(NE);
+  int* POSB =CNT;
   int* ESRC2=(int*)al(NE);
   int* EDST2=(int*)al(NE);
 
-  const size_t UNI = 28800000;
-  float* UN = al(UNI);
+  off = (off+3)&~(size_t)3;
+  unsigned short* QWA=(unsigned short*)al(1951744);
+  size_t qo=0;
+  auto qal=[&](size_t n)->unsigned short*{ unsigned short* p=QWA+qo; qo+=n; return p; };
+  unsigned short* q_degW1=qal(16384);
+  unsigned short* q_degW2=qal(8192);
+  unsigned short* q_degW3=qal(28672);
+  unsigned short* q_rW1=qal(131072);
+  unsigned short* q_rW2=qal(65536);
+  unsigned short* q_rW3=qal(229376);
+  unsigned short* q_WZ =qal(163840);
+  unsigned short* q_WF =qal(720896);
+  unsigned short* q_WG =qal(196608);
+  unsigned short* q_ff1=qal(1048576);
+  unsigned short* q_ff2=qal(1048576);
+  unsigned short* q_fW1=qal(65536);
+  unsigned short* q_fW2=qal(16384);
+  unsigned short* q_Wv1=qal(65536);
+  unsigned short* q_Wv2=qal(16384);
+  unsigned short* q_WaS=qal(32768);
+  unsigned short* q_WaD=qal(32768);
+  unsigned short* q_WaE=qal(16384);
+
+  float* outE=(float*)d_out;
+  float* outF=outE+NG;
+
+  size_t totalF = ws_size/sizeof(float);
+  if (off + 15500000 > totalF){
+    k_sentinel<<<G256(out_size)>>>(outE, out_size, (float)ws_size);
+    return;
+  }
+  size_t UNI = totalF - off;
+  float* UN = Wp + off;
+  int* PERMB = (int*)UN;
+
+  auto mkch=[&](size_t per, int& NCH, int& CH){
+    size_t c = UNI/per; if (c > (size_t)NE) c = NE;
+    NCH = (int)((NE + c - 1)/c);
+    CH  = (NE + NCH - 1)/NCH;
+  };
+  int NFd,CHFd, NBd,CHBd, NIFd,CHIFd, NIBd,CHIBd;
+  mkch(1088, NFd, CHFd);
+  mkch(1440, NBd, CHBd);
+  mkch(352,  NIFd, CHIFd);
+  mkch(928,  NIBd, CHIBd);
+
   float* TBc=UN;
   float* DTc=TBc+(size_t)NNC*512;
   float* P12=DTc+(size_t)NNC*512;
@@ -879,23 +939,31 @@
   float* DPb=V2 +(size_t)NN*160;
   float* F0N=DPb+(size_t)NN*96;
 
-  float* outE=(float*)d_out;
-  float* outF=outE+NG;
-
-  if (off*sizeof(float) > ws_size){
-    k_sentinel<<<G256(out_size)>>>(outE, out_size, (float)ws_size);
-    return;
-  }
-
   (void)hipMemsetAsync(CNT,0,NN*sizeof(int),stream);
   k_hist<<<G256(NE)>>>(edst,CNT,NE);
   k_scan0<<<dim3(1),dim3(256),0,stream>>>(CNT,ROWS);
   (void)hipMemcpyAsync(POSB,ROWS,NN*sizeof(int),hipMemcpyDeviceToDevice,stream);
   k_fillperm<<<G256(NE)>>>(edst,POSB,PERMB,NE);
   k_mkedge<<<G256(NE)>>>(PERMB,esrc,edst,ESRC2,EDST2);
-  k_wcat<<<G256(8*128*352)>>>(Wv0,Ws0,Ws1,Ws2,WCATF);
-  k_wcatz<<<G256(8*320*32)>>>(WaS,WaD,WaE,WCATZ);
-  k_wcatg<<<G256(8*128*96)>>>(fg1,fg2,WCATG);
+
+  k_qw<<<G256(8192)>>>(degW1,q_degW1,8192,8192);
+  k_qw<<<G256(4096)>>>(degW2,q_degW2,4096,4096);
+  k_qw<<<G256(14336)>>>(degW3,q_degW3,14336,14336);
+  k_qw<<<G256(65536)>>>(rW1,q_rW1,65536,65536);
+  k_qw<<<G256(32768)>>>(rW2,q_rW2,32768,32768);
+  k_qw<<<G256(114688)>>>(rW3,q_rW3,114688,114688);
+  k_qw<<<G256(524288)>>>(ff1,q_ff1,524288,524288);
+  k_qw<<<G256(524288)>>>(ff2,q_ff2,524288,524288);
+  k_qw<<<G256(32768)>>>(fW1,q_fW1,32768,32768);
+  k_qw<<<G256(8192)>>>(fW2,q_fW2,8192,8192);
+  k_qw<<<G256(32768)>>>(Wv1,q_Wv1,32768,32768);
+  k_qw<<<G256(8192)>>>(Wv2,q_Wv2,8192,8192);
+  k_qw<<<G256(32768)>>>(WaS,q_WaS,0,32768);
+  k_qw<<<G256(32768)>>>(WaD,q_WaD,0,32768);
+  k_qw<<<G256(16384)>>>(WaE,q_WaE,0,16384);
+  k_wcatfq<<<G256(8*128*352)>>>(Wv0,Ws0,Ws1,Ws2,q_WF);
+  k_wcatzq<<<G256(8*320*32)>>>(WaS,WaD,WaE,q_WZ);
+  k_wcatgq<<<G256(8*128*96)>>>(fg1,fg2,q_WG);
 
   k_geom<<<G256(NE)>>>(pos,ESRC2,EDST2,U,Rr,SH2b);
   k_f0init<<<G256(NN*128)>>>(natom,atab,FA0);
@@ -906,12 +974,12 @@
   (void)hipMemsetAsync(DPOS,0,(size_t)NN*3*4,stream);
 
   {
-    float* H1=UN; float* H2=H1+(size_t)CHIF*64; float* Gc=H2+(size_t)CHIF*64;
-    for (int cc=0;cc<NIF;cc++){
-      int c0e=cc*CHIF, cnt=(c0e+CHIF<=NE)?CHIF:(NE-c0e);
-      MG(64,false,false,1,false, true,true,false,false, Rr+c0e,nullptr,degW1,H1, cnt,64,128, rbfc,rbfw,nullptr,nullptr);
-      MGEMM3(64,false,false,1,false, H1,nullptr,degW2,H2, cnt,64,64);
-      MGEMM3(64,false,false,0,false, H2,nullptr,degW3,Gc, cnt,224,64);
+    float* H1=UN; float* H2=H1+(size_t)CHIFd*64; float* Gc=H2+(size_t)CHIFd*64;
+    for (int cc=0;cc<NIFd;cc++){
+      int c0e=cc*CHIFd, cnt=(c0e+CHIFd<=NE)?CHIFd:(NE-c0e);
+      MG(64,false,false,1,false, true,true,false,false, Rr+c0e,nullptr,q_degW1,8192,H1, cnt,64,128, rbfc,rbfw,nullptr,nullptr,nullptr);
+      MGEMM3(64,false,false,1,false, H1,nullptr,q_degW2,4096,H2, cnt,64,64);
+      MGEMM3(64,false,false,0,false, H2,nullptr,q_degW3,14336,Gc, cnt,224,64);
       k_agg<true><<<dim3(NG),dim3(512),0,stream>>>(FA0,FA1,FA2,
         nullptr,nullptr,nullptr, Gc,U,SH2b, nullptr, EDST2,EDST2, nullptr, c0e,c0e+cnt);
     }
@@ -922,46 +990,51 @@
 
   {
     float* H1  =UN;
-    float* H2  =H1  +(size_t)CHF*64;
-    float* Gc  =H2  +(size_t)CHF*64;
-    float* SCAT=Gc  +(size_t)CHF*224;
-    float* SV1 =SCAT+(size_t)CHF*352;
-    float* SV2 =SV1 +(size_t)CHF*192;
-    float* Zc  =SV2 +(size_t)CHF*160;
+    float* H2  =H1  +(size_t)CHFd*64;
+    float* Gc  =H2  +(size_t)CHFd*64;
+    float* SCAT=Gc  +(size_t)CHFd*224;
+    float* SV1 =SCAT+(size_t)CHFd*352;
+    float* SV2 =SV1 +(size_t)CHFd*192;
+    float* Zc  =SV2 +(size_t)CHFd*160;
     for (int i=0;i<8;i++){
-      const float* Wv1i=Wv1+(size_t)i*4096; const float* Wv2i=Wv2+(size_t)i*1024;
-      const float* rW1i=rW1+(size_t)i*8192; const float* rW2i=rW2+(size_t)i*4096; const float* rW3i=rW3+(size_t)i*14336;
-      const float* WZi=WCATZ+(size_t)i*10240;
-      const float* ff1i=ff1+(size_t)i*65536; const float* ff2i=ff2+(size_t)i*65536;
-      const float* fgCi=WCATG+(size_t)i*12288;
-      const float* fW1i=fW1+(size_t)i*4096; const float* fW2i=fW2+(size_t)i*1024;
-      const float* WCi=WCATF+(size_t)i*45056;
+      const unsigned short* rW1q=q_rW1+(size_t)i*8192;
+      const unsigned short* rW2q=q_rW2+(size_t)i*4096;
+      const unsigned short* rW3q=q_rW3+(size_t)i*14336;
+      const unsigned short* WZq =q_WZ +(size_t)i*10240;
+      const unsigned short* WCq =q_WF +(size_t)i*45056;
+      const unsigned short* ffq1=q_ff1+(size_t)i*65536;
+      const unsigned short* ffq2=q_ff2+(size_t)i*65536;
+      const unsigned short* fgq =q_WG +(size_t)i*12288;
+      const unsigned short* fW1q=q_fW1+(size_t)i*4096;
+      const unsigned short* fW2q=q_fW2+(size_t)i*1024;
+      const unsigned short* Wv1q=q_Wv1+(size_t)i*4096;
+      const unsigned short* Wv2q=q_Wv2+(size_t)i*1024;
       float* AB=ABLK+(size_t)i*NE;
 
       (void)hipMemsetAsync(SACC,0,(size_t)NN*4,stream);
       (void)hipMemsetAsync(n0_,0,(size_t)NN*128*4,stream);
       (void)hipMemsetAsync(n1_,0,(size_t)NN*352*4,stream);
-      for (int cc=0;cc<NF;cc++){
-        int c0e=cc*CHF, cnt=(c0e+CHF<=NE)?CHF:(NE-c0e);
-        MG(64,false,false,1,false, true,true,false,false, Rr+c0e,nullptr,rW1i,H1, cnt,64,128, rbfc,rbfw,nullptr,nullptr);
-        MGEMM3(64,false,false,1,false, H1,nullptr,rW2i,H2, cnt,64,64);
-        MGEMM3(64,false,false,0,false, H2,nullptr,rW3i,Gc, cnt,224,64);
+      for (int cc=0;cc<NFd;cc++){
+        int c0e=cc*CHFd, cnt=(c0e+CHFd<=NE)?CHFd:(NE-c0e);
+        MG(64,false,false,1,false, true,true,false,false, Rr+c0e,nullptr,rW1q,65536,H1, cnt,64,128, rbfc,rbfw,nullptr,nullptr,nullptr);
+        MGEMM3(64,false,false,1,false, H1,nullptr,rW2q,32768,H2, cnt,64,64);
+        MGEMM3(64,false,false,0,false, H2,nullptr,rW3q,114688,Gc, cnt,224,64);
         k_zgemm<true,true><<<dim3((unsigned)((cnt+63)/64)),dim3(256),0,stream>>>(
-            c0_, ESRC2+c0e, EDST2+c0e, H2, WZi, wab+(size_t)i*32, Zc, LAM+c0e, cnt);
-        MGEMM3(64,false,false,0,true, c0_,ESRC2+c0e,WCi,SCAT, cnt,352,128);
-        MEINS3(64,64,3,false,false,true, c1_,ESRC2+c0e,Wv1i,SV1, cnt);
-        MEINS3(32,32,5,false,false,true, c2_,ESRC2+c0e,Wv2i,SV2, cnt);
+            c0_, ESRC2+c0e, EDST2+c0e, H2, WZq, 81920, wab+(size_t)i*32, Zc, LAM+c0e, cnt);
+        MGEMM3(64,false,false,0,true, c0_,ESRC2+c0e,WCq,360448,SCAT, cnt,352,128);
+        MEINS3(64,64,3,false,false,true, c1_,ESRC2+c0e,Wv1q,32768,SV1, cnt);
+        MEINS3(32,32,5,false,false,true, c2_,ESRC2+c0e,Wv2q,8192,SV2, cnt);
         k_agg<false><<<dim3(NG),dim3(512),0,stream>>>(n0_,n1_,n2_,
           SCAT,SV1,SV2, Gc,U,SH2b, LAM, EDST2,EDST2, SACC, c0e,c0e+cnt);
       }
       k_postblk<<<G256(NN*480)>>>(c0_,c1_,c2_, n0_,n1_,n2_, SACC, CKB+(size_t)(i+1)*SLOT, LAM, EDST2, AB);
       for (int nc=0;nc<NN/NNC;nc++){
-        MGEMM3(64,false,false,1,false, n0_+(size_t)nc*NNC*128,nullptr,ff1i,TBc, NNC,512,128);
-        MGEMM3(64,false,true, 0,false, TBc,nullptr,ff2i, n0_+(size_t)nc*NNC*128, NNC,128,512);
-      }
-      MGEMM3(64,false,false,3,false, n0_,nullptr,fgCi,P12, NN,96,128);
-      MEINSG(64,64,3,true, n1_,fW1i,c1_, NN, P12, 0);
-      MEINSG(32,32,5,true, n2_,fW2i,c2_, NN, P12, 64);
+        MGEMM3(64,false,false,1,false, n0_+(size_t)nc*NNC*128,nullptr,ffq1,524288,TBc, NNC,512,128);
+        MGEMM3(64,false,true, 0,false, TBc,nullptr,ffq2,524288, n0_+(size_t)nc*NNC*128, NNC,128,512);
+      }
+      MGEMM3(64,false,false,3,false, n0_,nullptr,fgq,98304,P12, NN,96,128);
+      MEINSG(64,64,3,true, n1_,fW1q,32768,c1_, NN, P12, 0);
+      MEINSG(32,32,5,true, n2_,fW2q,8192,c2_, NN, P12, 64);
       float* t;
       t=c0_;c0_=n0_;n0_=t;
     }
@@ -972,91 +1045,96 @@
 
   {
     float* PRE1=UN;
-    float* PRE2=PRE1+(size_t)CHB*64;
-    float* H1  =PRE2+(size_t)CHB*64;
-    float* H2  =H1  +(size_t)CHB*64;
-    float* Gc  =H2  +(size_t)CHB*64;
-    float* DGc =Gc  +(size_t)CHB*224;
-    float* SCAT=DGc +(size_t)CHB*224;
-    float* SV1 =SCAT+(size_t)CHB*352;
-    float* SV2 =SV1 +(size_t)CHB*192;
-    float* Zc  =SV2 +(size_t)CHB*160;
+    float* PRE2=PRE1+(size_t)CHBd*64;
+    float* H1  =PRE2+(size_t)CHBd*64;
+    float* H2  =H1  +(size_t)CHBd*64;
+    float* Gc  =H2  +(size_t)CHBd*64;
+    float* DGc =Gc  +(size_t)CHBd*224;
+    float* SCAT=DGc +(size_t)CHBd*224;
+    float* SV1 =SCAT+(size_t)CHBd*352;
+    float* SV2 =SV1 +(size_t)CHBd*192;
+    float* Zc  =SV2 +(size_t)CHBd*160;
     float* DE0 =PRE1;
     float* RBFc=DGc;
     float* DZD =Gc;
     for (int i=7;i>=0;--i){
-      const float* Wv1i=Wv1+(size_t)i*4096; const float* Wv2i=Wv2+(size_t)i*1024;
-      const float* rW1i=rW1+(size_t)i*8192; const float* rW2i=rW2+(size_t)i*4096; const float* rW3i=rW3+(size_t)i*14336;
-      const float* WZi=WCATZ+(size_t)i*10240;
-      const float* WaSi=WaS+(size_t)i*4096; const float* WaDi=WaD+(size_t)i*4096; const float* WaEi=WaE+(size_t)i*2048;
-      const float* ff1i=ff1+(size_t)i*65536; const float* ff2i=ff2+(size_t)i*65536;
-      const float* fgCi=WCATG+(size_t)i*12288;
-      const float* fW1i=fW1+(size_t)i*4096; const float* fW2i=fW2+(size_t)i*1024;
-      const float* WCi=WCATF+(size_t)i*45056;
+      const unsigned short* rW1q=q_rW1+(size_t)i*8192;
+      const unsigned short* rW2q=q_rW2+(size_t)i*4096;
+      const unsigned short* rW3q=q_rW3+(size_t)i*14336;
+      const unsigned short* WZq =q_WZ +(size_t)i*10240;
+      const unsigned short* WCq =q_WF +(size_t)i*45056;
+      const unsigned short* ffq1=q_ff1+(size_t)i*65536;
+      const unsigned short* ffq2=q_ff2+(size_t)i*65536;
+      const unsigned short* fgq =q_WG +(size_t)i*12288;
+      const unsigned short* fW1q=q_fW1+(size_t)i*4096;
+      const unsigned short* fW2q=q_fW2+(size_t)i*1024;
+      const unsigned short* Wv1q=q_Wv1+(size_t)i*4096;
+      const unsigned short* Wv2q=q_Wv2+(size_t)i*1024;
+      const unsigned short* WaSq=q_WaS+(size_t)i*4096;
+      const unsigned short* WaDq=q_WaD+(size_t)i*4096;
+      const unsigned short* WaEq=q_WaE+(size_t)i*2048;
       const float* AB=ABLK+(size_t)i*NE;
       float *fa1=FA1, *fa2=FA2, *dy1=DY1, *dy2=DY2;
 
       k_dq3x2<<<G256(NN*480)>>>(CKB+(size_t)i*SLOT, CKB+(size_t)(i+1)*SLOT, FA0,FA1,FA2, FB0,FB1,FB2);
       if (i>0){
-        const float* pf1=ff1+(size_t)(i-1)*65536; const float* pf2=ff2+(size_t)(i-1)*65536;
-        const float* pgC=WCATG+(size_t)(i-1)*12288;
-        const float* pW1=fW1+(size_t)(i-1)*4096; const float* pW2=fW2+(size_t)(i-1)*1024;
+        const unsigned short* pfq1=q_ff1+(size_t)(i-1)*65536;
+        const unsigned short* pfq2=q_ff2+(size_t)(i-1)*65536;
+        const unsigned short* pgq =q_WG +(size_t)(i-1)*12288;
+        const unsigned short* pW1q=q_fW1+(size_t)(i-1)*4096;
+        const unsigned short* pW2q=q_fW2+(size_t)(i-1)*1024;
         for (int nc=0;nc<NN/NNC;nc++){
-          MGEMM(64,false,false,1,false, FA0+(size_t)nc*NNC*128,nullptr,pf1,TBc, NNC,512,128);
-          MGEMM(64,false,true, 0,false, TBc,nullptr,pf2, FA0+(size_t)nc*NNC*128, NNC,128,512);
+          MGEMM(64,false,false,1,false, FA0+(size_t)nc*NNC*128,nullptr,pfq1,524288,TBc, NNC,512,128);
+          MGEMM(64,false,true, 0,false, TBc,nullptr,pfq2,524288, FA0+(size_t)nc*NNC*128, NNC,128,512);
         }
-        MGEMM(64,false,false,3,false, FA0,nullptr,pgC,P12, NN,96,128);
-        MEINSG(64,64,3,false, FA1,pW1,DY1, NN, P12, 0);
-        MEINSG(32,32,5,false, FA2,pW2,DY2, NN, P12, 64);
+        MGEMM(64,false,false,3,false, FA0,nullptr,pgq,98304,P12, NN,96,128);
+        MEINSG(64,64,3,false, FA1,pW1q,32768,DY1, NN, P12, 0);
+        MEINSG(32,32,5,false, FA2,pW2q,8192,DY2, NN, P12, 64);
         fa1=DY1; dy1=FA1; fa2=DY2; dy2=FA2;
       }
-      (void)hipMemcpyAsync(F0N,FB0,(size_t)NN*128*4,hipMemcpyDeviceToDevice,stream);
       for (int nc=0;nc<NN/NNC;nc++){
-        MGEMM(64,false,false,1,false, FB0+(size_t)nc*NNC*128,nullptr,ff1i,TBc, NNC,512,128);
-        MGEMM(64,false,true, 0,false, TBc,nullptr,ff2i, F0N+(size_t)nc*NNC*128, NNC,128,512);
-      }
-      MGEMM(64,false,false,3,false, F0N,nullptr,fgCi,P12, NN,96,128);
-      MEINS(64,64,3,false,false,false, FB1,nullptr,fW1i,V1, NN);
-      MEINS(32,32,5,false,false,false, FB2,nullptr,fW2i,V2, NN);
+        MGEMM(64,false,false,1,false, FB0+(size_t)nc*NNC*128,nullptr,ffq1,524288,TBc, NNC,512,128);
+        MGEMMD(64,false,true, 0,false, TBc,nullptr,ffq2,524288, F0N+(size_t)nc*NNC*128, NNC,128,512, FB0+(size_t)nc*NNC*128);
+      }
+      MGEMM(64,false,false,3,false, F0N,nullptr,fgq,98304,P12, NN,96,128);
+      MEINS(64,64,3,false,false,false, FB1,nullptr,fW1q,32768,V1, NN);
+      MEINS(32,32,5,false,false,false, FB2,nullptr,fW2q,8192,V2, NN);
       k_gateback<64,3><<<G256(NN*64)>>>(DI1,V1,P12,DPb,0);
       k_gateback<32,5><<<G256(NN*32)>>>(DI2,V2,P12,DPb,64);
-      MGEMM(64,true,true,0,false, DPb,nullptr,fgCi,DI0, NN,128,96);
-      (void)hipMemcpyAsync(dy1,DI1,(size_t)NN*192*4,hipMemcpyDeviceToDevice,stream);
-      MEINS(64,64,3,true,true,false, V1,nullptr,fW1i,dy1, NN);
-      (void)hipMemcpyAsync(dy2,DI2,(size_t)NN*160*4,hipMemcpyDeviceToDevice,stream);
-      MEINS(32,32,5,true,true,false, V2,nullptr,fW2i,dy2, NN);
-      (void)hipMemcpyAsync(DY0,DI0,(size_t)NN*128*4,hipMemcpyDeviceToDevice,stream);
+      MGEMM(64,true,true,0,false, DPb,nullptr,fgq,98304,DI0, NN,128,96);
+      MEINSD(64,64,3,true,true,false, V1,nullptr,fW1q,32768,dy1, NN, DI1);
+      MEINSD(32,32,5,true,true,false, V2,nullptr,fW2q,8192,dy2, NN, DI2);
       for (int nc=0;nc<NN/NNC;nc++){
-        MGEMM(64,false,false,0,false, FB0+(size_t)nc*NNC*128,nullptr,ff1i,TBc, NNC,512,128);
-        MG(64,true,false,0,false, false,false,true,false, DI0+(size_t)nc*NNC*128,nullptr,ff2i,DTc, NNC,512,128, nullptr,nullptr,TBc,nullptr);
-        MGEMM(64,true,true,0,false, DTc,nullptr,ff1i, DY0+(size_t)nc*NNC*128, NNC,128,512);
+        MGEMM(64,false,false,0,false, FB0+(size_t)nc*NNC*128,nullptr,ffq1,524288,TBc, NNC,512,128);
+        MG(64,true,false,0,false, false,false,true,false, DI0+(size_t)nc*NNC*128,nullptr,ffq2,524288,DTc, NNC,512,128, nullptr,nullptr,TBc,nullptr,nullptr);
+        MGEMMD(64,true,true,0,false, DTc,nullptr,ffq1,524288, DY0+(size_t)nc*NNC*128, NNC,128,512, DI0+(size_t)nc*NNC*128);
       }
       k_ssum<<<dim3(NN/4),dim3(256),0,stream>>>(FA0,fa1,fa2,FB0,FB1,FB2,DY0,dy1,dy2,SSUM);
       (void)hipMemcpyAsync(DI0,DY0,(size_t)NN*128*4,hipMemcpyDeviceToDevice,stream);
       (void)hipMemcpyAsync(DI1,dy1,(size_t)NN*192*4,hipMemcpyDeviceToDevice,stream);
       (void)hipMemcpyAsync(DI2,dy2,(size_t)NN*160*4,hipMemcpyDeviceToDevice,stream);
-      for (int cc=0;cc<NB;cc++){
-        int c0e=cc*CHB, cnt=(c0e+CHB<=NE)?CHB:(NE-c0e);
-        MG(64,false,false,1,false, false,true,false,true, Rr+c0e,nullptr,rW1i,H1, cnt,64,128, rbfc,rbfw,nullptr,PRE1);
-        MG(64,false,false,1,false, false,false,false,true, H1,nullptr,rW2i,H2, cnt,64,64, nullptr,nullptr,nullptr,PRE2);
-        MGEMM(64,false,false,0,false, H2,nullptr,rW3i,Gc, cnt,224,64);
+      for (int cc=0;cc<NBd;cc++){
+        int c0e=cc*CHBd, cnt=(c0e+CHBd<=NE)?CHBd:(NE-c0e);
+        MG(64,false,false,1,false, false,true,false,true, Rr+c0e,nullptr,rW1q,65536,H1, cnt,64,128, rbfc,rbfw,nullptr,PRE1,nullptr);
+        MG(64,false,false,1,false, false,false,false,true, H1,nullptr,rW2q,32768,H2, cnt,64,64, nullptr,nullptr,nullptr,PRE2,nullptr);
+        MGEMM(64,false,false,0,false, H2,nullptr,rW3q,114688,Gc, cnt,224,64);
         k_zgemm<false,false><<<dim3((unsigned)((cnt+63)/64)),dim3(256),0,stream>>>(
-            FA0, ESRC2+c0e, EDST2+c0e, H2, WZi, nullptr, Zc, nullptr, cnt);
-        MGEMM(64,false,false,0,true, FA0,ESRC2+c0e,WCi,SCAT, cnt,352,128);
-        MEINS(64,64,3,false,false,true, fa1,ESRC2+c0e,Wv1i,SV1, cnt);
-        MEINS(32,32,5,false,false,true, fa2,ESRC2+c0e,Wv2i,SV2, cnt);
+            FA0, ESRC2+c0e, EDST2+c0e, H2, WZq, 81920, nullptr, Zc, nullptr, cnt);
+        MGEMM(64,false,false,0,true, FA0,ESRC2+c0e,WCq,360448,SCAT, cnt,352,128);
+        MEINS(64,64,3,false,false,true, fa1,ESRC2+c0e,Wv1q,32768,SV1, cnt);
+        MEINS(32,32,5,false,false,true, fa2,ESRC2+c0e,Wv2q,8192,SV2, cnt);
         k_bedge<<<GW4(cnt)>>>(SCAT,SV1,SV2, Gc,U,SH2b, DY0,dy1,dy2, EDST2, SSUM,
                               wab+(size_t)i*32, Zc, AB, DGc, DSH1, DSH2, c0e, cnt);
-        MGEMM(64,true,false,0,false, Zc,nullptr,WaEi,H2, cnt,64,32);
-        MG(64,true,true,0,false, false,false,true,false, DGc,nullptr,rW3i,H2, cnt,64,224, nullptr,nullptr,PRE2,nullptr);
-        MG(64,true,false,0,false, false,false,true,false, H2,nullptr,rW2i,H1, cnt,64,64, nullptr,nullptr,PRE1,nullptr);
-        MGEMM(64,true,false,0,false, H1,nullptr,rW1i,RBFc, cnt,128,64);
+        MGEMM(64,true,false,0,false, Zc,nullptr,WaEq,0,H2, cnt,64,32);
+        MG(64,true,true,0,false, false,false,true,false, DGc,nullptr,rW3q,114688,H2, cnt,64,224, nullptr,nullptr,PRE2,nullptr,nullptr);
+        MG(64,true,false,0,false, false,false,true,false, H2,nullptr,rW2q,32768,H1, cnt,64,64, nullptr,nullptr,PRE1,nullptr,nullptr);
+        MGEMM(64,true,false,0,false, H1,nullptr,rW1q,65536,RBFc, cnt,128,64);
         k_dr<<<GW4(cnt)>>>(RBFc,Rr,rbfc,rbfw,DRr, c0e,cnt);
-        MGEMM(64,true,false,0,false, SCAT,nullptr,WCi,DE0, cnt,128,352);
-        MGEMM(64,true,true, 0,false, Zc,nullptr,WaSi,DE0, cnt,128,32);
-        MGEMM(64,true,false,0,false, Zc,nullptr,WaDi,DZD, cnt,128,32);
-        MEINS(64,64,3,true,false,false, SV1,nullptr,Wv1i,SV1, cnt);
-        MEINS(32,32,5,true,false,false, SV2,nullptr,Wv2i,SV2, cnt);
+        MGEMM(64,true,false,0,false, SCAT,nullptr,WCq,360448,DE0, cnt,128,352);
+        MGEMM(64,true,true, 0,false, Zc,nullptr,WaSq,0,DE0, cnt,128,32);
+        MGEMM(64,true,false,0,false, Zc,nullptr,WaDq,0,DZD, cnt,128,32);
+        MEINS(64,64,3,true,false,false, SV1,nullptr,Wv1q,32768,SV1, cnt);
+        MEINS(32,32,5,true,false,false, SV2,nullptr,Wv2q,8192,SV2, cnt);
         k_scat<<<dim3(NG),dim3(640),0,stream>>>(DI0,DI1,DI2, DE0,DZD,SV1,SV2, ESRC2,EDST2, c0e,c0e+cnt);
       }
     }
@@ -1064,21 +1142,21 @@
 
   {
     float* PRE1=UN;
-    float* PRE2=PRE1+(size_t)CHIB*64;
-    float* H1  =PRE2+(size_t)CHIB*64;
-    float* H2  =H1  +(size_t)CHIB*64;
-    float* Gc  =H2  +(size_t)CHIB*64;
-    float* DGc =Gc  +(size_t)CHIB*224;
-    float* RBFc=DGc +(size_t)CHIB*224;
-    for (int cc=0;cc<NIB;cc++){
-      int c0e=cc*CHIB, cnt=(c0e+CHIB<=NE)?CHIB:(NE-c0e);
-      MG(64,false,false,1,false, false,true,false,true, Rr+c0e,nullptr,degW1,H1, cnt,64,128, rbfc,rbfw,nullptr,PRE1);
-      MG(64,false,false,1,false, false,false,false,true, H1,nullptr,degW2,H2, cnt,64,64, nullptr,nullptr,nullptr,PRE2);
-      MGEMM(64,false,false,0,false, H2,nullptr,degW3,Gc, cnt,224,64);
+    float* PRE2=PRE1+(size_t)CHIBd*64;
+    float* H1  =PRE2+(size_t)CHIBd*64;
+    float* H2  =H1  +(size_t)CHIBd*64;
+    float* Gc  =H2  +(size_t)CHIBd*64;
+    float* DGc =Gc  +(size_t)CHIBd*224;
+    float* RBFc=DGc +(size_t)CHIBd*224;
+    for (int cc=0;cc<NIBd;cc++){
+      int c0e=cc*CHIBd, cnt=(c0e+CHIBd<=NE)?CHIBd:(NE-c0e);
+      MG(64,false,false,1,false, false,true,false,true, Rr+c0e,nullptr,q_degW1,8192,H1, cnt,64,128, rbfc,rbfw,nullptr,PRE1,nullptr);
+      MG(64,false,false,1,false, false,false,false,true, H1,nullptr,q_degW2,4096,H2, cnt,64,64, nullptr,nullptr,nullptr,PRE2,nullptr);
+      MGEMM(64,false,false,0,false, H2,nullptr,q_degW3,14336,Gc, cnt,224,64);
       k_initback<<<GW4(cnt)>>>(DI0,DI1,DI2,EDST2,Gc,U,SH2b,DGc,DSH1,DSH2, c0e,cnt);
-      MG(64,true,false,0,false, false,false,true,false, DGc,nullptr,degW3,H2, cnt,64,224, nullptr,nullptr,PRE2,nullptr);
-      MG(64,true,false,0,false, false,false,true,false, H2,nullptr,degW2,H1, cnt,64,64, nullptr,nullptr,PRE1,nullptr);
-      MGEMM(64,true,false,0,false, H1,nullptr,degW1,RBFc, cnt,128,64);
+      MG(64,true,false,0,false, false,false,true,false, DGc,nullptr,q_degW3,14336,H2, cnt,64,224, nullptr,nullptr,PRE2,nullptr,nullptr);
+      MG(64,true,false,0,false, false,false,true,false, H2,nullptr,q_degW2,4096,H1, cnt,64,64, nullptr,nullptr,PRE1,nullptr,nullptr);
+      MGEMM(64,true,false,0,false, H1,nullptr,q_degW1,8192,RBFc, cnt,128,64);
       k_dr<<<GW4(cnt)>>>(RBFc,Rr,rbfc,rbfw,DRr, c0e,cnt);
     }
   }
```

New measurement: 33.38 ms. +5.7%, slower.
